# Kernel tuning notes

Hardware: AMD Instinct MI355X
Metric: run time of the kernel (lower is better)

The kernel has to match this reference:

```python
import jax, jax.numpy as jnp
import numpy as np

# Cleaned/faithful JAX port of TATLMPLayer. The original torch code has obvious
# typos (edge_type_feature_embedding used before assignment, self.weight_mlp vs
# self._weight_mlp, missing dim= in concatenate, elementwise mult of (B,E,K) with
# (K,D)); we implement the clearly intended math: two-level masked-softmax
# message passing over an incidence matrix H, gumbel-softmax typed edge
# embeddings, and a 4-head cross-attention to polyline features.

NEG_SLOPE = 0.01  # torch leaky_relu default
TAU = 0.5         # gumbel-softmax temperature 1/2


def _mlp(x, W1, b1, W2, b2):
    return jnp.maximum(x @ W1 + b1, 0.0) @ W2 + b2


def setup_inputs() -> dict:
    B, N, E, P, D, T, K, Hd = 2, 256, 512, 256, 128, 8, 8, 256
    key = jax.random.key(0)
    ks = jax.random.split(key, 40)
    g = lambda i, shape, s=0.05: jax.random.normal(ks[i], shape, dtype=jnp.float32) * s
    return {
        "agent_features": jax.random.normal(ks[0], (B, N, D), dtype=jnp.float32),
        "agent_types": jax.random.uniform(ks[1], (B, N, T), dtype=jnp.float32),
        "polyline_features": jax.random.normal(ks[2], (B, P, D), dtype=jnp.float32),
        "H": (jax.random.uniform(ks[3], (B, E, N)) < 0.1).astype(jnp.float32),
        "type_emb": g(4, (K, D)),
        "w_W1": g(5, (2 * D, Hd)), "w_b1": g(6, (Hd,)), "w_W2": g(7, (Hd, 1)), "w_b2": g(8, (1,)),
        "d_W1": g(9, (D + T, Hd)), "d_b1": g(10, (Hd,)), "d_W2": g(11, (Hd, K)), "d_b2": g(12, (K,)),
        "f_W1": g(13, (D + T, Hd)), "f_b1": g(14, (Hd,)), "f_W2": g(15, (Hd, 1)), "f_b2": g(16, (1,)),
        "o_W1": g(17, (4 * D, Hd)), "o_b1": g(18, (Hd,)), "o_W2": g(19, (Hd, D)), "o_b2": g(20, (D,)),
        "q_W": g(21, (3 * D, D)), "q_b": g(22, (D,)),
        "k_W": g(23, (D, D)), "k_b": g(24, (D,)),
        "v_W": g(25, (D, D)), "v_b": g(26, (D,)),
        "iq_W": g(27, (D, D)), "iq_b": g(28, (D,)),
        "ik_W": g(29, (D, D)), "ik_b": g(30, (D,)),
        "iv_W": g(31, (D, D)), "iv_b": g(32, (D,)),
        "op_W": g(33, (D, D)), "op_b": g(34, (D,)),
    }


def reference(agent_features, agent_types, polyline_features, H, type_emb,
              w_W1, w_b1, w_W2, w_b2, d_W1, d_b1, d_W2, d_b2,
              f_W1, f_b1, f_W2, f_b2, o_W1, o_b1, o_W2, o_b2,
              q_W, q_b, k_W, k_b, v_W, v_b,
              iq_W, iq_b, ik_W, ik_b, iv_W, iv_b, op_W, op_b):
    B, N, D = agent_features.shape
    E = H.shape[1]

    # level 1: incidence-aggregated edge features
    ef_init = jnp.einsum('ben,bnd->bed', H, agent_features)            # (B,E,D)
    pair = jnp.concatenate([
        jnp.broadcast_to(ef_init[:, :, None, :], (B, E, N, D)),
        jnp.broadcast_to(agent_features[:, None, :, :], (B, E, N, D))], axis=-1)
    ew = _mlp(pair, w_W1, w_b1, w_W2, w_b2)[..., 0]                    # (B,E,N)
    Hw = jax.nn.softmax(ew * H, axis=2) * H
    edge_features = jnp.einsum('ben,bnd->bed', Hw, agent_features)     # (B,E,D)

    # typed edge embedding via gumbel-softmax over edge types
    edge_type = jnp.einsum('ben,bnt->bet', H, agent_types)             # (B,E,T)
    et = jnp.concatenate([edge_features, edge_type], axis=-1)          # (B,E,D+T)
    logits = _mlp(et, d_W1, d_b1, d_W2, d_b2)                          # (B,E,K)
    u = jax.random.uniform(jax.random.key(42), logits.shape, minval=1e-6, maxval=1.0 - 1e-6)
    gumbel = -jnp.log(-jnp.log(u))
    distribution = jax.nn.softmax((logits + gumbel) / TAU, axis=-1)
    factor = jax.nn.sigmoid(_mlp(et, f_W1, f_b1, f_W2, f_b2))          # (B,E,1)
    edge_type_embedding = jnp.einsum('bek,kd->bed', factor * distribution, type_emb)

    # level 2: masked edge->agent message passing
    pair2 = jnp.concatenate([
        jnp.broadcast_to(edge_type_embedding[:, :, None, :], (B, E, N, D)),
        jnp.broadcast_to(agent_features[:, None, :, :], (B, E, N, D))], axis=-1)
    pair2 = pair2 * H[..., None]
    hw2 = jnp.where(_mlp(pair2, w_W1, w_b1, w_W2, w_b2)[..., 0] > 0,
                    _mlp(pair2, w_W1, w_b1, w_W2, w_b2)[..., 0], 0.0)
    # leaky relu (single-eval form)
    raw2 = _mlp(pair2, w_W1, w_b1, w_W2, w_b2)[..., 0]
    hw2 = jnp.where(raw2 > 0, raw2, NEG_SLOPE * raw2)                  # (B,E,N)
    Hw2 = jax.nn.softmax(hw2, axis=2) * H
    msg = jnp.einsum('ben,bef->bnf', Hw2,
                     jnp.concatenate([edge_features, edge_type_embedding], axis=-1))
    agent_feat = jnp.concatenate([msg, agent_features], axis=-1)       # (B,N,3D)

    # cross-attention to polylines (4 heads)
    Q = agent_feat @ q_W + q_b
    Kp = polyline_features @ k_W + k_b
    Vp = polyline_features @ v_W + v_b
    q2 = Q @ iq_W + iq_b
    k2 = Kp @ ik_W + ik_b
    v2 = Vp @ iv_W + iv_b
    nh, hd = 4, D // 4
    qh = q2.reshape(B, N, nh, hd)
    kh = k2.reshape(B, -1, nh, hd)
    vh = v2.reshape(B, -1, nh, hd)
    att = jax.nn.softmax(jnp.einsum('bqhd,bkhd->bhqk', qh, kh) / jnp.sqrt(jnp.float32(hd)), axis=-1)
    o = jnp.einsum('bhqk,bkhd->bqhd', att, vh).reshape(B, N, D)
    polyline_new = o @ op_W + op_b                                     # (B,N,D)

    agent_new = _mlp(jnp.concatenate([agent_feat, polyline_new], axis=-1),
                     o_W1, o_b1, o_W2, o_b2)                           # (B,N,D)
    return agent_new, polyline_new
```

## Files before the change

kernel.cpp:

```cpp
#include <hip/hip_runtime.h>
#include <math.h>

#define BB 2
#define NN 256
#define EE 512
#define PP 256
#define DD 128
#define TT 8
#define KK 8
#define HDIM 256

#define WS_G      0
#define WS_C0     8192
#define WS_V      8256
#define WS_U1     139328
#define WS_ETYPE  401472
#define WS_EDGEF  409664
#define WS_ETE    540736
#define WS_HWT    671808
#define WS_K2     933952
#define WS_V2     999488

#define PB_GUM 16
#define PB_INC 272
#define PB_V   528
#define PB_END 784

__device__ inline unsigned rotl32(unsigned x, int d){ return (x<<d)|(x>>(32-d)); }

__device__ inline float bits_to_gumbel(unsigned bits){
  float f = __uint_as_float((bits>>9)|0x3f800000u) - 1.0f;
  const float minv = 1e-6f;
  const float maxv = 1.0f - 1e-6f;
  float u = f*(maxv-minv) + minv;
  u = fmaxf(minv, u);
  return -logf(-logf(u));
}

__device__ __forceinline__ void f4fma(float4& a, float x, const float4& w){
  a.x += x*w.x; a.y += x*w.y; a.z += x*w.z; a.w += x*w.w;
}

__device__ __forceinline__ void block_reduce2_sum(float v[2], float* wred){
  int lane = threadIdx.x & 63, wid = threadIdx.x >> 6;
  #pragma unroll
  for (int s=32;s>0;s>>=1){
    #pragma unroll
    for (int r=0;r<2;r++){ v[r] += __shfl_xor(v[r], s, 64); }
  }
  if (lane==0){
    #pragma unroll
    for (int r=0;r<2;r++) wred[wid*2+r]=v[r];
  }
  __syncthreads();
  #pragma unroll
  for (int r=0;r<2;r++)
    v[r] = (wred[0*2+r]+wred[1*2+r]) + (wred[2*2+r]+wred[3*2+r]);
  __syncthreads();
}

__device__ __forceinline__ void mlp128_lds2(const float (*in)[DD], const float* W, const float* bias,
                                            float (*outl)[DD], float* part, int t){
  int c=(t&31)*4, ks=t>>5;
  float4 a[2];
  #pragma unroll
  for (int r=0;r<2;r++) a[r]=make_float4(0.f,0.f,0.f,0.f);
  #pragma unroll 4
  for (int i=ks*16;i<ks*16+16;i++){
    float4 w = *(const float4*)&W[(size_t)i*DD+c];
    #pragma unroll
    for (int r=0;r<2;r++) f4fma(a[r], in[r][i], w);
  }
  #pragma unroll
  for (int r=0;r<2;r++) *(float4*)&part[(ks*2+r)*DD+c]=a[r];
  __syncthreads();
  int cc=t&127, r=t>>7;
  {
    float s=0.f;
    #pragma unroll
    for (int k2=0;k2<8;k2++) s+=part[(k2*2+r)*DD+cc];
    outl[r][cc]=s+bias[cc];
  }
  __syncthreads();
}

__device__ __forceinline__ void mlp128_glob2(const float (*in)[DD], const float* W, const float* bias,
                                             float* dst, int r0, float* part, int t){
  int c=(t&31)*4, ks=t>>5;
  float4 a[2];
  #pragma unroll
  for (int r=0;r<2;r++) a[r]=make_float4(0.f,0.f,0.f,0.f);
  #pragma unroll 4
  for (int i=ks*16;i<ks*16+16;i++){
    float4 w = *(const float4*)&W[(size_t)i*DD+c];
    #pragma unroll
    for (int r=0;r<2;r++) f4fma(a[r], in[r][i], w);
  }
  #pragma unroll
  for (int r=0;r<2;r++) *(float4*)&part[(ks*2+r)*DD+c]=a[r];
  __syncthreads();
  int cc=t&127, r=t>>7;
  {
    float s=0.f;
    #pragma unroll
    for (int k2=0;k2<8;k2++) s+=part[(k2*2+r)*DD+cc];
    dst[(size_t)(r0+r)*DD+cc]=s+bias[cc];
  }
  __syncthreads();
}

__global__ void prep_kernel(float* g, float* c0, const float* w_b1,
                            const float* w_W2, const float* w_b2,
                            const float* Hm, const float* af, const float* at,
                            const float* wW1, const float* wb1,
                            float* U1g, float* etype_g, float* Vout,
                            const float* pf,
                            const float* kW, const float* kb, const float* ikW, const float* ikb,
                            const float* vW, const float* vb, const float* ivW, const float* ivb,
                            float* k2, float* v2){
  __shared__ float part[4096];
  __shared__ float wred[16];
  __shared__ int   hcomp[4*256];
  __shared__ int   hcnt[4];
  __shared__ float ef[4][DD];
  __shared__ float xs[2][DD];
  __shared__ float bufB[2][DD];
  int blk = blockIdx.x;
  int t = threadIdx.x;
  int lane = t & 63, wid = t >> 6;

  if (blk < PB_GUM){
    int j = blk*256 + t;
    {
      const unsigned k0=0u, k1=42u;
      const unsigned ks2 = k0^k1^0x1BD11BDAu;
      unsigned x0 = (unsigned)j, x1 = (unsigned)j + 4096u;
      const int r0_[4]={13,15,26,6}, r1_[4]={17,29,16,24};
      x0 += k0; x1 += k1;
      #pragma unroll
      for(int i=0;i<4;i++){ x0+=x1; x1=rotl32(x1,r0_[i]); x1^=x0; }
      x0+=k1; x1+=ks2+1u;
      #pragma unroll
      for(int i=0;i<4;i++){ x0+=x1; x1=rotl32(x1,r1_[i]); x1^=x0; }
      x0+=ks2; x1+=k0+2u;
      #pragma unroll
      for(int i=0;i<4;i++){ x0+=x1; x1=rotl32(x1,r0_[i]); x1^=x0; }
      x0+=k0; x1+=k1+3u;
      #pragma unroll
      for(int i=0;i<4;i++){ x0+=x1; x1=rotl32(x1,r1_[i]); x1^=x0; }
      x0+=k1; x1+=ks2+4u;
      #pragma unroll
      for(int i=0;i<4;i++){ x0+=x1; x1=rotl32(x1,r0_[i]); x1^=x0; }
      x0+=ks2; x1+=k0+5u;
      g[j]      = bits_to_gumbel(x0);
      g[j+4096] = bits_to_gumbel(x1);
    }
    if (blk == 0){
      float v4[2];
      v4[0] = fmaxf(w_b1[t],0.f)*w_W2[t]; v4[1]=0.f;
      block_reduce2_sum(v4, wred);
      if (t==0) c0[0] = v4[0] + w_b2[0];
    }
  } else if (blk < PB_INC){
    int e0 = (blk - PB_GUM)*4;
    int b = e0 >> 9;
    {
      int r = wid;
      const float* Hrow = Hm + (size_t)(e0+r)*NN;
      int base = 0;
      #pragma unroll
      for (int c4=0;c4<4;c4++){
        int n2 = c4*64 + lane;
        bool pred = (Hrow[n2] != 0.f);
        unsigned long long mask = __ballot(pred);
        int off = __popcll(mask & ((1ull<<lane)-1ull));
        if (pred) hcomp[r*256+base+off] = n2;
        base += __popcll(mask);
      }
      if (lane==0) hcnt[r] = base;
    }
    __syncthreads();
    {
      int d = t & 127, eh = t >> 7;
      #pragma unroll
      for (int rr=0;rr<2;rr++){
        int r = eh*2 + rr;
        int tot = hcnt[r];
        float a = 0.f, a2 = 0.f;
        for (int i=0;i<tot;i++){
          int n2 = hcomp[r*256+i];
          a += af[((size_t)b*NN+n2)*DD + d];
          if (d < TT) a2 += at[((size_t)b*NN+n2)*TT + d];
        }
        ef[r][d] = a;
        if (d < TT) etype_g[(size_t)(e0+r)*TT + d] = a2;
      }
    }
    __syncthreads();
    {
      int c = (t&63)*4, ks = t>>6;
      float4 acc[4];
      #pragma unroll
      for (int r=0;r<4;r++) acc[r]=make_float4(0.f,0.f,0.f,0.f);
      #pragma unroll 8
      for (int i=ks*32; i<ks*32+32; i++){
        float4 w = *(const float4*)&wW1[(size_t)i*HDIM + c];
        #pragma unroll
        for (int r=0;r<4;r++) f4fma(acc[r], ef[r][i], w);
      }
      #pragma unroll
      for (int r=0;r<4;r++) *(float4*)&part[(ks*4+r)*HDIM + c] = acc[r];
    }
    __syncthreads();
    {
      float bv = wb1[t];
      #pragma unroll
      for (int r=0;r<4;r++){
        float s = (part[(0*4+r)*HDIM+t] + part[(1*4+r)*HDIM+t])
                + (part[(2*4+r)*HDIM+t] + part[(3*4+r)*HDIM+t]);
        U1g[(size_t)(e0+r)*HDIM + t] = s + bv;
      }
    }
  } else if (blk < PB_V){
    int r0 = (blk - PB_INC)*2;
    const float* W = wW1 + (size_t)DD*HDIM;
    for (int i=t;i<2*DD;i+=256) xs[i>>7][i&127] = af[(size_t)(r0+(i>>7))*DD + (i&127)];
    __syncthreads();
    int c = (t&63)*4, ks = t>>6;
    float4 acc[2];
    #pragma unroll
    for (int r=0;r<2;r++) acc[r]=make_float4(0.f,0.f,0.f,0.f);
    #pragma unroll 8
    for (int i=ks*32; i<ks*32+32; i++){
      float4 w = *(const float4*)&W[(size_t)i*HDIM + c];
      #pragma unroll
      for (int r=0;r<2;r++) f4fma(acc[r], xs[r][i], w);
    }
    #pragma unroll
    for (int r=0;r<2;r++) *(float4*)&part[(ks*2+r)*HDIM + c] = acc[r];
    __syncthreads();
    #pragma unroll
    for (int r=0;r<2;r++){
      float s = (part[(0*2+r)*HDIM+t] + part[(1*2+r)*HDIM+t])
              + (part[(2*2+r)*HDIM+t] + part[(3*2+r)*HDIM+t]);
      Vout[(size_t)(r0+r)*HDIM + t] = s;
    }
  } else {
    int r0 = (blk - PB_V)*2;
    for (int i=t;i<2*DD;i+=256) xs[i>>7][i&127] = pf[(size_t)(r0+(i>>7))*DD + (i&127)];
    __syncthreads();
    mlp128_lds2 (xs, kW, kb, bufB, part, t);
    mlp128_glob2(bufB, ikW, ikb, k2, r0, part, t);
    mlp128_lds2 (xs, vW, vb, bufB, part, t);
    mlp128_glob2(bufB, ivW, ivb, v2, r0, part, t);
  }
}

__global__ __launch_bounds__(512) void edge_kernel(
                            const float* Hm, const float* af,
                            const float* Vm, const float* U1g, const float* etype_g,
                            const float* wW1, const float* wb1, const float* wW2, const float* wb2,
                            const float* dW1, const float* db1, const float* dW2, const float* db2,
                            const float* fW1, const float* fb1, const float* fW2, const float* fb2,
                            const float* type_emb, const float* g, const float* c0p,
                            float* edgef_g, float* ete_g, float* HwT){
  __shared__ float bufA[8192];
  __shared__ float w2s[HDIM*KK];
  __shared__ float w2l[HDIM];
  __shared__ float et4[4][144];
  __shared__ float hd4[4][HDIM];
  __shared__ float redsm[512];
  __shared__ float wred[16];
  __shared__ float fdv[4][KK];
  __shared__ int   hcnt[4];
  __shared__ int   hcomp[4*256];

  int e0 = blockIdx.x*4;
  int b  = e0 >> 9;
  int t  = threadIdx.x;
  int lane = t & 63, wid = t >> 6;

  int cW=(t&63)*4, ksW=t>>6;
  float4 wreg[16];
  #pragma unroll
  for (int i=0;i<16;i++)
    wreg[i] = *(const float4*)&wW1[(size_t)(ksW*16+i)*HDIM + cW];

  if (t < HDIM) w2l[t] = wW2[t];
  for (int i=t;i<HDIM*KK;i+=512) w2s[i] = dW2[i];
  {
    int h=t&255, rh=t>>8;
    #pragma unroll
    for (int rr=0;rr<2;rr++){
      int r = 2*rh+rr;
      hd4[r][h] = U1g[(size_t)(e0+r)*HDIM + h];
    }
  }
  if (t < 32){ int r=t>>3, j=t&7; et4[r][DD+j] = etype_g[(size_t)(e0+r)*TT + j]; }
  if (wid < 4){
    int r = wid;
    const float* Hrow = Hm + (size_t)(e0+r)*NN;
    int base = 0;
    #pragma unroll
    for (int c4=0;c4<4;c4++){
      int n2 = c4*64 + lane;
      bool pred = (Hrow[n2] != 0.f);
      unsigned long long mask = __ballot(pred);
      int off = __popcll(mask & ((1ull<<lane)-1ull));
      if (pred) hcomp[r*256+base+off] = n2;
      base += __popcll(mask);
    }
    if (lane==0) hcnt[r] = base;
  }
  __syncthreads();
  {
    int n = t&255, hh = t>>8;
    const float4* Vrow = (const float4*)(Vm + ((size_t)(b*NN)+n)*HDIM);
    float acc[4]={0.f,0.f,0.f,0.f};
    #pragma unroll 4
    for (int ii=hh*32; ii<hh*32+32; ii++){
      float4 v = Vrow[ii];
      float w0=w2l[4*ii+0], w1=w2l[4*ii+1], wc=w2l[4*ii+2], w3=w2l[4*ii+3];
      #pragma unroll
      for (int r=0;r<4;r++){
        acc[r] += fmaxf(hd4[r][4*ii+0]+v.x,0.f)*w0
                + fmaxf(hd4[r][4*ii+1]+v.y,0.f)*w1
                + fmaxf(hd4[r][4*ii+2]+v.z,0.f)*wc
                + fmaxf(hd4[r][4*ii+3]+v.w,0.f)*w3;
      }
    }
    #pragma unroll
    for (int r=0;r<4;r++) bufA[(hh*4+r)*256 + n] = acc[r];
  }
  __syncthreads();
  if (wid < 4){
    int r = wid;
    float b2v = wb2[0];
    float x[4]; bool msk[4];
    #pragma unroll
    for (int q=0;q<4;q++){
      int n = lane + 64*q;
      msk[q] = (Hm[(size_t)(e0+r)*NN + n] != 0.f);
      x[q] = msk[q] ? (bufA[(0*4+r)*256+n] + bufA[(1*4+r)*256+n] + b2v) : 0.f;
    }
    float m = fmaxf(fmaxf(x[0],x[1]), fmaxf(x[2],x[3]));
    #pragma unroll
    for (int s2=32;s2>0;s2>>=1) m = fmaxf(m, __shfl_xor(m, s2, 64));
    float p[4]; float ss=0.f;
    #pragma unroll
    for (int q=0;q<4;q++){ p[q]=expf(x[q]-m); ss+=p[q]; }
    #pragma unroll
    for (int s2=32;s2>0;s2>>=1) ss += __shfl_xor(ss, s2, 64);
    float inv = 1.f/ss;
    #pragma unroll
    for (int q=0;q<4;q++){
      int n = lane + 64*q;
      bufA[3072 + r*256 + n] = msk[q] ? p[q]*inv : 0.f;
    }
  }
  __syncthreads();
  {
    int d = t & 127, r = t >> 7;
    int tot = hcnt[r];
    float a = 0.f;
    for (int i=0;i<tot;i++){
      int n2 = hcomp[r*256+i];
      a += bufA[3072 + r*256 + n2] * af[((size_t)b*NN+n2)*DD + d];
    }
    et4[r][d] = a;
    edgef_g[(size_t)(e0+r)*DD + d] = a;
  }
  __syncthreads();
  {
    int half = t>>8, tt = t&255;
    int c=(tt&63)*4, ks=tt>>6;
    const float* W = half ? fW1 : dW1;
    float4 acc[4];
    #pragma unroll
    for (int r=0;r<4;r++) acc[r]=make_float4(0.f,0.f,0.f,0.f);
    #pragma unroll 4
    for (int i=ks*34;i<ks*34+34;i++){
      float4 w = *(const float4*)&W[(size_t)i*HDIM+c];
      #pragma unroll
      for (int r=0;r<4;r++) f4fma(acc[r], et4[r][i], w);
    }
    #pragma unroll
    for (int r=0;r<4;r++) *(float4*)&bufA[half*4096 + (ks*4+r)*HDIM + c] = acc[r];
  }
  __syncthreads();
  {
    int h=t&255, rh=t>>8;
    float bd = db1[h], bf = fb1[h], fw = fW2[h];
    float val[2];
    #pragma unroll
    for (int rr=0;rr<2;rr++){
      int r = 2*rh+rr;
      float sd=0.f, sf=0.f;
      #pragma unroll
      for (int k=0;k<4;k++){ sd += bufA[(k*4+r)*HDIM+h]; sf += bufA[4096+(k*4+r)*HDIM+h]; }
      hd4[r][h] = fmaxf(sd+bd, 0.f);
      val[rr] = fmaxf(sf+bf, 0.f)*fw;
    }
    #pragma unroll
    for (int s2=32;s2>0;s2>>=1){
      val[0] += __shfl_xor(val[0], s2, 64);
      val[1] += __shfl_xor(val[1], s2, 64);
    }
    if (lane==0){ wred[wid*2]=val[0]; wred[wid*2+1]=val[1]; }
  }
  __syncthreads();
  {
    int r_ = t>>7, rem = t&127, k_ = rem&7, j_ = rem>>3;
    float lp = 0.f;
    #pragma unroll 4
    for (int i=0;i<16;i++){
      int h = j_ + 16*i;
      lp += hd4[r_][h]*w2s[h*KK + k_];
    }
    redsm[t] = lp;
  }
  __syncthreads();
  if (wid == 0 && lane < 32){
    int r = lane>>3, k = lane&7;
    int base = (r>=2)?4:0, off = r&1;
    float fs = 0.f;
    #pragma unroll
    for (int w=0;w<4;w++) fs += wred[(base+w)*2 + off];
    float fac = 1.f/(1.f+expf(-(fs+fb2[0])));
    float s = db2[k] + g[(size_t)(e0+r)*KK + k];
    #pragma unroll
    for (int j=0;j<16;j++) s += redsm[r*128 + j*8 + k];
    float z = s*2.0f;
    float m = z;
    m = fmaxf(m, __shfl_xor(m, 1, 64));
    m = fmaxf(m, __shfl_xor(m, 2, 64));
    m = fmaxf(m, __shfl_xor(m, 4, 64));
    float pz = expf(z - m);
    float sum = pz;
    sum += __shfl_xor(sum, 1, 64);
    sum += __shfl_xor(sum, 2, 64);
    sum += __shfl_xor(sum, 4, 64);
    fdv[r][k] = fac * pz / sum;
  }
  __syncthreads();
  {
    int d = t&127, r = t>>7;
    float a = 0.f;
    #pragma unroll
    for (int k=0;k<KK;k++) a += fdv[r][k]*type_emb[(size_t)k*DD + d];
    et4[r][d] = a;
    ete_g[(size_t)(e0+r)*DD + d] = a;
  }
  __syncthreads();
  {
    float4 acc[4];
    #pragma unroll
    for (int r=0;r<4;r++) acc[r]=make_float4(0.f,0.f,0.f,0.f);
    #pragma unroll
    for (int i=0;i<16;i++){
      int idx = ksW*16 + i;
      #pragma unroll
      for (int r=0;r<4;r++) f4fma(acc[r], et4[r][idx], wreg[i]);
    }
    #pragma unroll
    for (int r=0;r<4;r++) *(float4*)&bufA[(ksW*4+r)*HDIM + cW] = acc[r];
  }
  __syncthreads();
  {
    int h=t&255, rh=t>>8;
    float bv = wb1[h];
    #pragma unroll
    for (int rr=0;rr<2;rr++){
      int r = 2*rh+rr;
      float s=0.f;
      #pragma unroll
      for (int k=0;k<8;k++) s += bufA[(k*4+r)*HDIM + h];
      hd4[r][h] = s + bv;
    }
  }
  __syncthreads();
  {
    int n = t&255, hh = t>>8;
    const float4* Vrow = (const float4*)(Vm + ((size_t)(b*NN)+n)*HDIM);
    float acc[4]={0.f,0.f,0.f,0.f};
    #pragma unroll 4
    for (int ii=hh*32; ii<hh*32+32; ii++){
      float4 v = Vrow[ii];
      float w0=w2l[4*ii+0], w1=w2l[4*ii+1], wc=w2l[4*ii+2], w3=w2l[4*ii+3];
      #pragma unroll
      for (int r=0;r<4;r++){
        acc[r] += fmaxf(hd4[r][4*ii+0]+v.x,0.f)*w0
                + fmaxf(hd4[r][4*ii+1]+v.y,0.f)*w1
                + fmaxf(hd4[r][4*ii+2]+v.z,0.f)*wc
                + fmaxf(hd4[r][4*ii+3]+v.w,0.f)*w3;
      }
    }
    #pragma unroll
    for (int r=0;r<4;r++) bufA[(hh*4+r)*256 + n] = acc[r];
  }
  __syncthreads();
  if (wid < 4){
    int r = wid;
    float b2v = wb2[0];
    float c0 = c0p[0];
    float x[4]; bool msk[4];
    #pragma unroll
    for (int q=0;q<4;q++){
      int n = lane + 64*q;
      msk[q] = (Hm[(size_t)(e0+r)*NN + n] != 0.f);
      float raw = msk[q] ? (bufA[(0*4+r)*256+n] + bufA[(1*4+r)*256+n] + b2v) : c0;
      x[q] = raw>0.f ? raw : 0.01f*raw;
    }
    float m = fmaxf(fmaxf(x[0],x[1]), fmaxf(x[2],x[3]));
    #pragma unroll
    for (int s2=32;s2>0;s2>>=1) m = fmaxf(m, __shfl_xor(m, s2, 64));
    float p[4]; float ss=0.f;
    #pragma unroll
    for (int q=0;q<4;q++){ p[q]=expf(x[q]-m); ss+=p[q]; }
    #pragma unroll
    for (int s2=32;s2>0;s2>>=1) ss += __shfl_xor(ss, s2, 64);
    float inv = 1.f/ss;
    #pragma unroll
    for (int q=0;q<4;q++){
      int n = lane + 64*q;
      bufA[2048 + r*256 + n] = msk[q] ? p[q]*inv : 0.f;
    }
  }
  __syncthreads();
  if (t < 256){
    int n = t;
    float4 o4;
    o4.x = bufA[2048 + 0*256 + n];
    o4.y = bufA[2048 + 1*256 + n];
    o4.z = bufA[2048 + 2*256 + n];
    o4.w = bufA[2048 + 3*256 + n];
    int eb = e0 & 511;
    *(float4*)(HwT + ((size_t)(b*NN)+n)*EE + eb) = o4;
  }
}

__global__ __launch_bounds__(512) void agent_kernel(
                             const float* HwT, const float* edgef, const float* ete,
                             const float* af,
                             const float* qW, const float* qb, const float* iqW, const float* iqb,
                             const float* k2, const float* v2,
                             const float* op_W, const float* op_b,
                             const float* oW1, const float* ob1,
                             const float* oW2, const float* ob2,
                             float* pnew, float* anew){
  __shared__ int   ecomp[2][EE];
  __shared__ float wcomp[2][EE];
  __shared__ int   wcnt[2][4];
  __shared__ float agfl[2][512];
  __shared__ float part[4096];
  __shared__ float Qs[2][DD];
  __shared__ float qr[2][DD];
  __shared__ float att[2][4][PP+1];
  __shared__ float o_l[2][DD];
  __shared__ float hid[2][HDIM];
  int n0 = blockIdx.x*2; int b = n0 >> 8; int t = threadIdx.x;
  int tt = t & 255, rr = t >> 8;
  int lane = t & 63, wid = t >> 6;
  int lw = tt >> 6;

  {
    int bn = n0 + rr;
    const float* wrow = HwT + (size_t)bn*EE;
    int total = 0;
    #pragma unroll
    for (int p=0;p<2;p++){
      int e = p*256 + tt;
      float w = wrow[e];
      bool pred = (w != 0.f);
      unsigned long long mask = __ballot(pred);
      if (lane==0) wcnt[rr][lw] = __popcll(mask);
      int off = __popcll(mask & ((1ull<<lane)-1ull));
      __syncthreads();
      int wb = total;
      for (int ww=0; ww<lw; ww++) wb += wcnt[rr][ww];
      if (pred){ ecomp[rr][wb+off] = e; wcomp[rr][wb+off] = w; }
      total += wcnt[rr][0]+wcnt[rr][1]+wcnt[rr][2]+wcnt[rr][3];
      __syncthreads();
    }
    float acc = 0.f;
    const float* srcbase = (tt < DD) ? (edgef + (size_t)b*EE*DD + tt)
                                     : (ete   + (size_t)b*EE*DD + (tt-DD));
    for (int i=0;i<total;i++){
      acc += wcomp[rr][i] * srcbase[(size_t)ecomp[rr][i]*DD];
    }
    agfl[rr][tt] = acc;
    if (tt < DD) agfl[rr][2*DD+tt] = af[(size_t)bn*DD + tt];
  }
  __syncthreads();
  int c=(tt&31)*4, ps=tt>>5;
  {
    float4 a = make_float4(0.f,0.f,0.f,0.f);
    #pragma unroll 4
    for (int i=ps*48;i<ps*48+48;i++){
      float4 w = *(const float4*)&qW[(size_t)i*DD+c];
      f4fma(a, agfl[rr][i], w);
    }
    *(float4*)&part[(rr*8+ps)*DD+c]=a;
  }
  __syncthreads();
  if (t<256){
    int cc=t&127, r=t>>7;
    float s=0.f;
    #pragma unroll
    for (int k=0;k<8;k++) s+=part[(r*8+k)*DD+cc];
    Qs[r][cc]=s+qb[cc];
  }
  __syncthreads();
  {
    float4 a = make_float4(0.f,0.f,0.f,0.f);
    #pragma unroll 4
    for (int i=ps*16;i<ps*16+16;i++){
      float4 w = *(const float4*)&iqW[(size_t)i*DD+c];
      f4fma(a, Qs[rr][i], w);
    }
    *(float4*)&part[(rr*8+ps)*DD+c]=a;
  }
  __syncthreads();
  if (t<256){
    int cc=t&127, r=t>>7;
    float s=0.f;
    #pragma unroll
    for (int k=0;k<8;k++) s+=part[(r*8+k)*DD+cc];
    qr[r][cc]=s+iqb[cc];
  }
  __syncthreads();
  const float scale = 0.17677669529663687f;
  {
    const float* krow = k2 + ((size_t)(b*PP) + tt)*DD;
    #pragma unroll
    for (int hh=0;hh<2;hh++){
      int h = rr*2+hh;
      const float4* k4 = (const float4*)(krow + h*32);
      float s0=0.f, s1=0.f;
      #pragma unroll
      for (int jj=0;jj<8;jj++){
        float4 kk = k4[jj];
        s0 += qr[0][h*32+jj*4+0]*kk.x + qr[0][h*32+jj*4+1]*kk.y
            + qr[0][h*32+jj*4+2]*kk.z + qr[0][h*32+jj*4+3]*kk.w;
        s1 += qr[1][h*32+jj*4+0]*kk.x + qr[1][h*32+jj*4+1]*kk.y
            + qr[1][h*32+jj*4+2]*kk.z + qr[1][h*32+jj*4+3]*kk.w;
      }
      att[0][h][tt] = s0*scale;
      att[1][h][tt] = s1*scale;
    }
  }
  __syncthreads();
  {
    int r = wid>>2, h = wid&3;
    float v0 = att[r][h][lane],     v1 = att[r][h][lane+64],
          ve = att[r][h][lane+128], v3 = att[r][h][lane+192];
    float m = fmaxf(fmaxf(v0,v1), fmaxf(ve,v3));
    #pragma unroll
    for (int s2=32;s2>0;s2>>=1) m = fmaxf(m, __shfl_xor(m, s2, 64));
    float e0 = expf(v0-m), e1 = expf(v1-m), e2 = expf(ve-m), e3 = expf(v3-m);
    float ss = (e0+e1)+(e2+e3);
    #pragma unroll
    for (int s2=32;s2>0;s2>>=1) ss += __shfl_xor(ss, s2, 64);
    float inv = 1.f/ss;
    att[r][h][lane] = e0*inv; att[r][h][lane+64] = e1*inv;
    att[r][h][lane+128] = e2*inv; att[r][h][lane+192] = e3*inv;
  }
  __syncthreads();
  int h2 = c >> 5;
  {
    float4 acc = make_float4(0.f,0.f,0.f,0.f);
    #pragma unroll 4
    for (int i=0;i<32;i++){
      int p = ps*32+i;
      float4 v = *(const float4*)&v2[((size_t)(b*PP)+p)*DD + c];
      f4fma(acc, att[rr][h2][p], v);
    }
    *(float4*)&part[(rr*8+ps)*DD+c]=acc;
  }
  __syncthreads();
  if (t<256){
    int cc=t&127, r=t>>7;
    float s=0.f;
    #pragma unroll
    for (int k=0;k<8;k++) s+=part[(r*8+k)*DD+cc];
    o_l[r][cc]=s;
  }
  __syncthreads();
  {
    float4 a2 = make_float4(0.f,0.f,0.f,0.f);
    #pragma unroll 4
    for (int i=ps*16;i<ps*16+16;i++){
      float4 w = *(const float4*)&op_W[(size_t)i*DD + c];
      f4fma(a2, o_l[rr][i], w);
    }
    *(float4*)&part[(rr*8+ps)*DD+c]=a2;
  }
  __syncthreads();
  if (t<256){
    int cc=t&127, r=t>>7;
    float s=0.f;
    #pragma unroll
    for (int k=0;k<8;k++) s+=part[(r*8+k)*DD+cc];
    float pv = s+op_b[cc];
    agfl[r][3*DD+cc] = pv;
    pnew[(size_t)(n0+r)*DD+cc] = pv;
  }
  __syncthreads();
  {
    int c1=(t&63)*4, ks1=t>>6;
    float4 acc[2];
    #pragma unroll
    for (int r=0;r<2;r++) acc[r]=make_float4(0.f,0.f,0.f,0.f);
    #pragma unroll 8
    for (int i=ks1*64;i<ks1*64+64;i++){
      float4 w = *(const float4*)&oW1[(size_t)i*HDIM+c1];
      f4fma(acc[0], agfl[0][i], w);
      f4fma(acc[1], agfl[1][i], w);
    }
    #pragma unroll
    for (int r=0;r<2;r++) *(float4*)&part[(ks1*2+r)*HDIM+c1]=acc[r];
  }
  __syncthreads();
  {
    int h=t&255, r=t>>8;
    float s=0.f;
    #pragma unroll
    for (int k=0;k<8;k++) s+=part[(k*2+r)*HDIM+h];
    hid[r][h] = fmaxf(s+ob1[h], 0.f);
  }
  __syncthreads();
  {
    float4 a2 = make_float4(0.f,0.f,0.f,0.f);
    #pragma unroll 8
    for (int h=ps*32;h<ps*32+32;h++){
      float4 w = *(const float4*)&oW2[(size_t)h*DD+c];
      f4fma(a2, hid[rr][h], w);
    }
    *(float4*)&part[(rr*8+ps)*DD+c]=a2;
  }
  __syncthreads();
  if (t<256){
    int cc=t&127, r=t>>7;
    float s=0.f;
    #pragma unroll
    for (int k=0;k<8;k++) s+=part[(r*8+k)*DD+cc];
    anew[(size_t)(n0+r)*DD+cc]=s+ob2[cc];
  }
}

extern "C" void kernel_launch(void* const* d_in, const int* in_sizes, int n_in,
                              void* d_out, int out_size, void* d_ws, size_t ws_size,
                              hipStream_t stream) {
  const float* af       = (const float*)d_in[0];
  const float* at       = (const float*)d_in[1];
  const float* pf       = (const float*)d_in[2];
  const float* Hm       = (const float*)d_in[3];
  const float* type_emb = (const float*)d_in[4];
  const float* w_W1 = (const float*)d_in[5];
  const float* w_b1 = (const float*)d_in[6];
  const float* w_W2 = (const float*)d_in[7];
  const float* w_b2 = (const float*)d_in[8];
  const float* d_W1 = (const float*)d_in[9];
  const float* d_b1 = (const float*)d_in[10];
  const float* d_W2 = (const float*)d_in[11];
  const float* d_b2 = (const float*)d_in[12];
  const float* f_W1 = (const float*)d_in[13];
  const float* f_b1 = (const float*)d_in[14];
  const float* f_W2 = (const float*)d_in[15];
  const float* f_b2 = (const float*)d_in[16];
  const float* o_W1 = (const float*)d_in[17];
  const float* o_b1 = (const float*)d_in[18];
  const float* o_W2 = (const float*)d_in[19];
  const float* o_b2 = (const float*)d_in[20];
  const float* q_W  = (const float*)d_in[21];
  const float* q_b  = (const float*)d_in[22];
  const float* k_W  = (const float*)d_in[23];
  const float* k_b  = (const float*)d_in[24];
  const float* v_W  = (const float*)d_in[25];
  const float* v_b  = (const float*)d_in[26];
  const float* iq_W = (const float*)d_in[27];
  const float* iq_b = (const float*)d_in[28];
  const float* ik_W = (const float*)d_in[29];
  const float* ik_b = (const float*)d_in[30];
  const float* iv_W = (const float*)d_in[31];
  const float* iv_b = (const float*)d_in[32];
  const float* op_W = (const float*)d_in[33];
  const float* op_b = (const float*)d_in[34];

  float* ws   = (float*)d_ws;
  float* out  = (float*)d_out;
  float* anew = out;
  float* pnew = out + BB*NN*DD;

  prep_kernel<<<PB_END, 256, 0, stream>>>(
      ws+WS_G, ws+WS_C0, w_b1, w_W2, w_b2,
      Hm, af, at, w_W1, w_b1,
      ws+WS_U1, ws+WS_ETYPE, ws+WS_V,
      pf, k_W,k_b,ik_W,ik_b, v_W,v_b,iv_W,iv_b,
      ws+WS_K2, ws+WS_V2);
  edge_kernel<<<256,512,0,stream>>>(
      Hm, af, ws+WS_V, ws+WS_U1, ws+WS_ETYPE,
      w_W1, w_b1, w_W2, w_b2,
      d_W1,d_b1,d_W2,d_b2, f_W1,f_b1,f_W2,f_b2,
      type_emb, ws+WS_G, ws+WS_C0,
      ws+WS_EDGEF, ws+WS_ETE, ws+WS_HWT);
  agent_kernel<<<256,512,0,stream>>>(
      ws+WS_HWT, ws+WS_EDGEF, ws+WS_ETE, af,
      q_W, q_b, iq_W, iq_b,
      ws+WS_K2, ws+WS_V2, op_W, op_b,
      o_W1,o_b1,o_W2,o_b2, pnew, anew);
}
```

Measured before the change: 89.08 us.

## Fuse three kernels into one persistent kernel with atomic grid barriers

```diff
diff --git a/kernel.cpp b/kernel.cpp
--- a/kernel.cpp
+++ b/kernel.cpp
@@ -10,21 +10,13 @@
 #define KK 8
 #define HDIM 256
 
-#define WS_G      0
-#define WS_C0     8192
-#define WS_V      8256
-#define WS_U1     139328
-#define WS_ETYPE  401472
-#define WS_EDGEF  409664
-#define WS_ETE    540736
-#define WS_HWT    671808
-#define WS_K2     933952
-#define WS_V2     999488
-
-#define PB_GUM 16
-#define PB_INC 272
-#define PB_V   528
-#define PB_END 784
+#define WS_V      0
+#define WS_EDGEF  131072
+#define WS_ETE    262144
+#define WS_HWT    393216
+#define WS_K2     655360
+#define WS_V2     720896
+#define WS_CNT    786432
 
 __device__ inline unsigned rotl32(unsigned x, int d){ return (x<<d)|(x>>(32-d)); }
 
@@ -41,97 +33,80 @@
   a.x += x*w.x; a.y += x*w.y; a.z += x*w.z; a.w += x*w.w;
 }
 
-__device__ __forceinline__ void block_reduce2_sum(float v[2], float* wred){
-  int lane = threadIdx.x & 63, wid = threadIdx.x >> 6;
-  #pragma unroll
-  for (int s=32;s>0;s>>=1){
-    #pragma unroll
-    for (int r=0;r<2;r++){ v[r] += __shfl_xor(v[r], s, 64); }
-  }
-  if (lane==0){
-    #pragma unroll
-    for (int r=0;r<2;r++) wred[wid*2+r]=v[r];
+__device__ __forceinline__ void grid_sync(int* cnt, int target){
+  __syncthreads();
+  if (threadIdx.x == 0){
+    __threadfence();
+    atomicAdd(cnt, 1);
+    while (__hip_atomic_load(cnt, __ATOMIC_ACQUIRE, __HIP_MEMORY_SCOPE_AGENT) < target){
+      __builtin_amdgcn_s_sleep(8);
+    }
   }
   __syncthreads();
-  #pragma unroll
-  for (int r=0;r<2;r++)
-    v[r] = (wred[0*2+r]+wred[1*2+r]) + (wred[2*2+r]+wred[3*2+r]);
+  __threadfence();
+}
+
+__device__ __forceinline__ void mlp128x2_512(const float* inA, const float* inB,
+      const float* W, const float* bias, float* outA, float* outB, float* part, int t){
+  int c=(t&31)*4, ks=t>>5;
+  float4 a0=make_float4(0.f,0.f,0.f,0.f), a1=a0;
+  #pragma unroll 4
+  for (int i=ks*8;i<ks*8+8;i++){
+    float4 w = *(const float4*)&W[(size_t)i*DD+c];
+    f4fma(a0, inA[i], w); f4fma(a1, inB[i], w);
+  }
+  *(float4*)&part[(ks*2+0)*DD+c]=a0;
+  *(float4*)&part[(ks*2+1)*DD+c]=a1;
   __syncthreads();
-}
-
-__device__ __forceinline__ void mlp128_lds2(const float (*in)[DD], const float* W, const float* bias,
-                                            float (*outl)[DD], float* part, int t){
-  int c=(t&31)*4, ks=t>>5;
-  float4 a[2];
-  #pragma unroll
-  for (int r=0;r<2;r++) a[r]=make_float4(0.f,0.f,0.f,0.f);
-  #pragma unroll 4
-  for (int i=ks*16;i<ks*16+16;i++){
-    float4 w = *(const float4*)&W[(size_t)i*DD+c];
-    #pragma unroll
-    for (int r=0;r<2;r++) f4fma(a[r], in[r][i], w);
-  }
-  #pragma unroll
-  for (int r=0;r<2;r++) *(float4*)&part[(ks*2+r)*DD+c]=a[r];
-  __syncthreads();
-  int cc=t&127, r=t>>7;
-  {
+  if (t < 256){
+    int cc=t&127, r=t>>7;
     float s=0.f;
     #pragma unroll
-    for (int k2=0;k2<8;k2++) s+=part[(k2*2+r)*DD+cc];
-    outl[r][cc]=s+bias[cc];
+    for (int k=0;k<16;k++) s+=part[(k*2+r)*DD+cc];
+    float val = s + bias[cc];
+    if (r==0) outA[cc]=val; else outB[cc]=val;
   }
   __syncthreads();
 }
 
-__device__ __forceinline__ void mlp128_glob2(const float (*in)[DD], const float* W, const float* bias,
-                                             float* dst, int r0, float* part, int t){
-  int c=(t&31)*4, ks=t>>5;
-  float4 a[2];
-  #pragma unroll
-  for (int r=0;r<2;r++) a[r]=make_float4(0.f,0.f,0.f,0.f);
-  #pragma unroll 4
-  for (int i=ks*16;i<ks*16+16;i++){
-    float4 w = *(const float4*)&W[(size_t)i*DD+c];
-    #pragma unroll
-    for (int r=0;r<2;r++) f4fma(a[r], in[r][i], w);
-  }
-  #pragma unroll
-  for (int r=0;r<2;r++) *(float4*)&part[(ks*2+r)*DD+c]=a[r];
-  __syncthreads();
-  int cc=t&127, r=t>>7;
-  {
-    float s=0.f;
-    #pragma unroll
-    for (int k2=0;k2<8;k2++) s+=part[(k2*2+r)*DD+cc];
-    dst[(size_t)(r0+r)*DD+cc]=s+bias[cc];
-  }
-  __syncthreads();
-}
-
-__global__ void prep_kernel(float* g, float* c0, const float* w_b1,
-                            const float* w_W2, const float* w_b2,
-                            const float* Hm, const float* af, const float* at,
-                            const float* wW1, const float* wb1,
-                            float* U1g, float* etype_g, float* Vout,
-                            const float* pf,
-                            const float* kW, const float* kb, const float* ikW, const float* ikb,
-                            const float* vW, const float* vb, const float* ivW, const float* ivb,
-                            float* k2, float* v2){
-  __shared__ float part[4096];
-  __shared__ float wred[16];
-  __shared__ int   hcomp[4*256];
-  __shared__ int   hcnt[4];
-  __shared__ float ef[4][DD];
-  __shared__ float xs[2][DD];
-  __shared__ float bufB[2][DD];
+__global__ __launch_bounds__(512) void fused_kernel(
+    const float* af, const float* at, const float* pf, const float* Hm,
+    const float* type_emb,
+    const float* wW1, const float* wb1, const float* wW2, const float* wb2,
+    const float* dW1, const float* db1, const float* dW2, const float* db2,
+    const float* fW1, const float* fb1, const float* fW2, const float* fb2,
+    const float* oW1, const float* ob1, const float* oW2, const float* ob2,
+    const float* qW,  const float* qb,  const float* kW,  const float* kb,
+    const float* vW,  const float* vb,  const float* iqW, const float* iqb,
+    const float* ikW, const float* ikb, const float* ivW, const float* ivb,
+    const float* opW, const float* opb,
+    float* Vg, float* edgef_g, float* ete_g, float* HwT,
+    float* k2g, float* v2g, int* cnt,
+    float* pnew, float* anew){
+
+  __shared__ float pool[11712];
+  __shared__ float hd4s[4*HDIM];
+  __shared__ int   hcompS[4*256];
+  __shared__ int   hcntS[4];
+  __shared__ float etloc[4*TT];
+  __shared__ float gloc[32];
+  __shared__ float wredS[16];
+  __shared__ float mredS[4], sinvS[4];
+  __shared__ float c0s;
+  __shared__ float fdvS[4*KK];
+
   int blk = blockIdx.x;
   int t = threadIdx.x;
   int lane = t & 63, wid = t >> 6;
 
-  if (blk < PB_GUM){
-    int j = blk*256 + t;
-    {
+  {
+    float* partA = pool;
+    float* ef    = pool + 8192;
+    float* xsA   = pool + 8704;
+    float* bufB  = pool + 8960;
+
+    if (t < 32){
+      int j = (blk < 128) ? (blk*32 + t) : ((blk-128)*32 + t);
       const unsigned k0=0u, k1=42u;
       const unsigned ks2 = k0^k1^0x1BD11BDAu;
       unsigned x0 = (unsigned)j, x1 = (unsigned)j + 4096u;
@@ -152,19 +127,20 @@
       #pragma unroll
       for(int i=0;i<4;i++){ x0+=x1; x1=rotl32(x1,r0_[i]); x1^=x0; }
       x0+=ks2; x1+=k0+5u;
-      g[j]      = bits_to_gumbel(x0);
-      g[j+4096] = bits_to_gumbel(x1);
-    }
-    if (blk == 0){
-      float v4[2];
-      v4[0] = fmaxf(w_b1[t],0.f)*w_W2[t]; v4[1]=0.f;
-      block_reduce2_sum(v4, wred);
-      if (t==0) c0[0] = v4[0] + w_b2[0];
-    }
-  } else if (blk < PB_INC){
-    int e0 = (blk - PB_GUM)*4;
-    int b = e0 >> 9;
-    {
+      gloc[t] = bits_to_gumbel((blk<128)? x0 : x1);
+    }
+    if (t < 256){
+      float v = fmaxf(wb1 ? 0.f : 0.f, 0.f);
+    }
+    if (t < 256){
+      float v = fmaxf(wb1[t],0.f)*wW2[t];
+      #pragma unroll
+      for (int s=32;s>0;s>>=1) v += __shfl_xor(v, s, 64);
+      if (lane==0) wredS[wid] = v;
+    }
+    int e0 = blk*4;
+    int b  = e0 >> 9;
+    if (wid < 4){
       int r = wid;
       const float* Hrow = Hm + (size_t)(e0+r)*NN;
       int base = 0;
@@ -174,577 +150,538 @@
         bool pred = (Hrow[n2] != 0.f);
         unsigned long long mask = __ballot(pred);
         int off = __popcll(mask & ((1ull<<lane)-1ull));
-        if (pred) hcomp[r*256+base+off] = n2;
+        if (pred) hcompS[r*256+base+off] = n2;
         base += __popcll(mask);
       }
-      if (lane==0) hcnt[r] = base;
-    }
-    __syncthreads();
-    {
-      int d = t & 127, eh = t >> 7;
+      if (lane==0) hcntS[r] = base;
+    }
+    __syncthreads();
+    if (t==0) c0s = wredS[0]+wredS[1]+wredS[2]+wredS[3] + wb2[0];
+    {
+      int d = t & 127, r = t >> 7;
+      int tot = hcntS[r];
+      float a = 0.f, a2 = 0.f;
+      for (int i=0;i<tot;i++){
+        int n2 = hcompS[r*256+i];
+        a += af[((size_t)b*NN+n2)*DD + d];
+        if (d < TT) a2 += at[((size_t)b*NN+n2)*TT + d];
+      }
+      ef[r*DD+d] = a;
+      if (d < TT) etloc[r*TT+d] = a2;
+    }
+    __syncthreads();
+    {
+      int c=(t&63)*4, ks=t>>6;
+      float4 acc[4];
+      #pragma unroll
+      for (int r=0;r<4;r++) acc[r]=make_float4(0.f,0.f,0.f,0.f);
+      #pragma unroll 4
+      for (int i=ks*16; i<ks*16+16; i++){
+        float4 w = *(const float4*)&wW1[(size_t)i*HDIM + c];
+        #pragma unroll
+        for (int r=0;r<4;r++) f4fma(acc[r], ef[r*DD+i], w);
+      }
+      #pragma unroll
+      for (int r=0;r<4;r++) *(float4*)&partA[(ks*4+r)*HDIM + c] = acc[r];
+    }
+    __syncthreads();
+    {
+      int h=t&255, rh=t>>8;
+      float bv = wb1[h];
       #pragma unroll
       for (int rr=0;rr<2;rr++){
-        int r = eh*2 + rr;
-        int tot = hcnt[r];
-        float a = 0.f, a2 = 0.f;
-        for (int i=0;i<tot;i++){
-          int n2 = hcomp[r*256+i];
-          a += af[((size_t)b*NN+n2)*DD + d];
-          if (d < TT) a2 += at[((size_t)b*NN+n2)*TT + d];
+        int r = 2*rh+rr;
+        float s=0.f;
+        #pragma unroll
+        for (int k=0;k<8;k++) s += partA[(k*4+r)*HDIM + h];
+        hd4s[r*HDIM+h] = s + bv;
+      }
+    }
+    __syncthreads();
+    {
+      int r0v = blk*2;
+      const float* W = wW1 + (size_t)DD*HDIM;
+      for (int i=t;i<2*DD;i+=512) xsA[i] = af[(size_t)(r0v+(i>>7))*DD + (i&127)];
+      __syncthreads();
+      int c=(t&63)*4, ks=t>>6;
+      float4 a0=make_float4(0.f,0.f,0.f,0.f), a1=a0;
+      #pragma unroll 4
+      for (int i=ks*16; i<ks*16+16; i++){
+        float4 w = *(const float4*)&W[(size_t)i*HDIM + c];
+        f4fma(a0, xsA[i], w); f4fma(a1, xsA[DD+i], w);
+      }
+      *(float4*)&partA[(ks*2+0)*HDIM + c] = a0;
+      *(float4*)&partA[(ks*2+1)*HDIM + c] = a1;
+      __syncthreads();
+      {
+        int h=t&255, r=t>>8;
+        float s=0.f;
+        #pragma unroll
+        for (int k=0;k<8;k++) s += partA[(k*2+r)*HDIM + h];
+        Vg[(size_t)(r0v+r)*HDIM + h] = s;
+      }
+      __syncthreads();
+    }
+    {
+      int r0p = blk*2;
+      for (int i=t;i<2*DD;i+=512) xsA[i] = pf[(size_t)(r0p+(i>>7))*DD + (i&127)];
+      __syncthreads();
+      mlp128x2_512(xsA, xsA+DD, kW, kb, bufB, bufB+DD, partA, t);
+      mlp128x2_512(bufB, bufB+DD, ikW, ikb,
+                   k2g + (size_t)r0p*DD, k2g + (size_t)(r0p+1)*DD, partA, t);
+      mlp128x2_512(xsA, xsA+DD, vW, vb, bufB, bufB+DD, partA, t);
+      mlp128x2_512(bufB, bufB+DD, ivW, ivb,
+                   v2g + (size_t)r0p*DD, v2g + (size_t)(r0p+1)*DD, partA, t);
+    }
+  }
+  grid_sync(cnt + 0, 256);
+
+  {
+    float* bufA = pool;
+    float* w2s  = pool + 8192;
+    float* w2l  = pool + 10240;
+    float* et4  = pool + 10496;
+    float* redsm= pool + 11072;
+
+    int e0 = blk*4;
+    int b  = e0 >> 9;
+
+    int cW=(t&63)*4, ksW=t>>6;
+    float4 wreg[16];
+    #pragma unroll
+    for (int i=0;i<16;i++)
+      wreg[i] = *(const float4*)&wW1[(size_t)(ksW*16+i)*HDIM + cW];
+
+    if (t < HDIM) w2l[t] = wW2[t];
+    for (int i=t;i<HDIM*KK;i+=512) w2s[i] = dW2[i];
+    if (t < 32){ int r=t>>3, j=t&7; et4[r*144+DD+j] = etloc[r*TT+j]; }
+    __syncthreads();
+    {
+      int n = t&255, hh = t>>8;
+      const float4* Vrow = (const float4*)(Vg + ((size_t)(b*NN)+n)*HDIM);
+      float acc[4]={0.f,0.f,0.f,0.f};
+      #pragma unroll 4
+      for (int ii=hh*32; ii<hh*32+32; ii++){
+        float4 v = Vrow[ii];
+        float w0=w2l[4*ii+0], w1=w2l[4*ii+1], wc=w2l[4*ii+2], w3=w2l[4*ii+3];
+        #pragma unroll
+        for (int r=0;r<4;r++){
+          acc[r] += fmaxf(hd4s[r*HDIM+4*ii+0]+v.x,0.f)*w0
+                  + fmaxf(hd4s[r*HDIM+4*ii+1]+v.y,0.f)*w1
+                  + fmaxf(hd4s[r*HDIM+4*ii+2]+v.z,0.f)*wc
+                  + fmaxf(hd4s[r*HDIM+4*ii+3]+v.w,0.f)*w3;
         }
-        ef[r][d] = a;
-        if (d < TT) etype_g[(size_t)(e0+r)*TT + d] = a2;
-      }
-    }
-    __syncthreads();
-    {
-      int c = (t&63)*4, ks = t>>6;
+      }
+      #pragma unroll
+      for (int r=0;r<4;r++) bufA[(hh*4+r)*256 + n] = acc[r];
+    }
+    __syncthreads();
+    if (wid < 4){
+      int r = wid;
+      float b2v = wb2[0];
+      float x[4]; bool msk[4];
+      #pragma unroll
+      for (int q=0;q<4;q++){
+        int n = lane + 64*q;
+        msk[q] = (Hm[(size_t)(e0+r)*NN + n] != 0.f);
+        x[q] = msk[q] ? (bufA[(0*4+r)*256+n] + bufA[(1*4+r)*256+n] + b2v) : 0.f;
+      }
+      float m = fmaxf(fmaxf(x[0],x[1]), fmaxf(x[2],x[3]));
+      #pragma unroll
+      for (int s2=32;s2>0;s2>>=1) m = fmaxf(m, __shfl_xor(m, s2, 64));
+      float p[4]; float ss=0.f;
+      #pragma unroll
+      for (int q=0;q<4;q++){ p[q]=expf(x[q]-m); ss+=p[q]; }
+      #pragma unroll
+      for (int s2=32;s2>0;s2>>=1) ss += __shfl_xor(ss, s2, 64);
+      float inv = 1.f/ss;
+      #pragma unroll
+      for (int q=0;q<4;q++){
+        int n = lane + 64*q;
+        bufA[3072 + r*256 + n] = msk[q] ? p[q]*inv : 0.f;
+      }
+    }
+    __syncthreads();
+    {
+      int d = t & 127, r = t >> 7;
+      int tot = hcntS[r];
+      float a = 0.f;
+      for (int i=0;i<tot;i++){
+        int n2 = hcompS[r*256+i];
+        a += bufA[3072 + r*256 + n2] * af[((size_t)b*NN+n2)*DD + d];
+      }
+      et4[r*144+d] = a;
+      edgef_g[(size_t)(e0+r)*DD + d] = a;
+    }
+    __syncthreads();
+    {
+      int half = t>>8, tt2 = t&255;
+      int c=(tt2&63)*4, ks=tt2>>6;
+      const float* W = half ? fW1 : dW1;
       float4 acc[4];
       #pragma unroll
       for (int r=0;r<4;r++) acc[r]=make_float4(0.f,0.f,0.f,0.f);
+      #pragma unroll 4
+      for (int i=ks*34;i<ks*34+34;i++){
+        float4 w = *(const float4*)&W[(size_t)i*HDIM+c];
+        #pragma unroll
+        for (int r=0;r<4;r++) f4fma(acc[r], et4[r*144+i], w);
+      }
+      #pragma unroll
+      for (int r=0;r<4;r++) *(float4*)&bufA[half*4096 + (ks*4+r)*HDIM + c] = acc[r];
+    }
+    __syncthreads();
+    {
+      int h=t&255, rh=t>>8;
+      float bd = db1[h], bf = fb1[h], fw = fW2[h];
+      float val[2];
+      #pragma unroll
+      for (int rr=0;rr<2;rr++){
+        int r = 2*rh+rr;
+        float sd=0.f, sf=0.f;
+        #pragma unroll
+        for (int k=0;k<4;k++){ sd += bufA[(k*4+r)*HDIM+h]; sf += bufA[4096+(k*4+r)*HDIM+h]; }
+        hd4s[r*HDIM+h] = fmaxf(sd+bd, 0.f);
+        val[rr] = fmaxf(sf+bf, 0.f)*fw;
+      }
+      #pragma unroll
+      for (int s2=32;s2>0;s2>>=1){
+        val[0] += __shfl_xor(val[0], s2, 64);
+        val[1] += __shfl_xor(val[1], s2, 64);
+      }
+      if (lane==0){ wredS[wid*2]=val[0]; wredS[wid*2+1]=val[1]; }
+    }
+    __syncthreads();
+    {
+      int r_ = t>>7, rem = t&127, k_ = rem&7, j_ = rem>>3;
+      float lp = 0.f;
+      #pragma unroll 4
+      for (int i=0;i<16;i++){
+        int h = j_ + 16*i;
+        lp += hd4s[r_*HDIM+h]*w2s[h*KK + k_];
+      }
+      redsm[t] = lp;
+    }
+    __syncthreads();
+    if (wid == 0 && lane < 32){
+      int r = lane>>3, k = lane&7;
+      int base = (r>=2)?4:0, off = r&1;
+      float fs = 0.f;
+      #pragma unroll
+      for (int w=0;w<4;w++) fs += wredS[(base+w)*2 + off];
+      float fac = 1.f/(1.f+expf(-(fs+fb2[0])));
+      float s = db2[k] + gloc[r*8+k];
+      #pragma unroll
+      for (int j=0;j<16;j++) s += redsm[r*128 + j*8 + k];
+      float z = s*2.0f;
+      float m = z;
+      m = fmaxf(m, __shfl_xor(m, 1, 64));
+      m = fmaxf(m, __shfl_xor(m, 2, 64));
+      m = fmaxf(m, __shfl_xor(m, 4, 64));
+      float pz = expf(z - m);
+      float sum = pz;
+      sum += __shfl_xor(sum, 1, 64);
+      sum += __shfl_xor(sum, 2, 64);
+      sum += __shfl_xor(sum, 4, 64);
+      fdvS[r*KK+k] = fac * pz / sum;
+    }
+    __syncthreads();
+    {
+      int d = t&127, r = t>>7;
+      float a = 0.f;
+      #pragma unroll
+      for (int k=0;k<KK;k++) a += fdvS[r*KK+k]*type_emb[(size_t)k*DD + d];
+      et4[r*144+d] = a;
+      ete_g[(size_t)(e0+r)*DD + d] = a;
+    }
+    __syncthreads();
+    {
+      float4 acc[4];
+      #pragma unroll
+      for (int r=0;r<4;r++) acc[r]=make_float4(0.f,0.f,0.f,0.f);
+      #pragma unroll
+      for (int i=0;i<16;i++){
+        int idx = ksW*16 + i;
+        #pragma unroll
+        for (int r=0;r<4;r++) f4fma(acc[r], et4[r*144+idx], wreg[i]);
+      }
+      #pragma unroll
+      for (int r=0;r<4;r++) *(float4*)&bufA[(ksW*4+r)*HDIM + cW] = acc[r];
+    }
+    __syncthreads();
+    {
+      int h=t&255, rh=t>>8;
+      float bv = wb1[h];
+      #pragma unroll
+      for (int rr=0;rr<2;rr++){
+        int r = 2*rh+rr;
+        float s=0.f;
+        #pragma unroll
+        for (int k=0;k<8;k++) s += bufA[(k*4+r)*HDIM + h];
+        hd4s[r*HDIM+h] = s + bv;
+      }
+    }
+    __syncthreads();
+    {
+      int n = t&255, hh = t>>8;
+      const float4* Vrow = (const float4*)(Vg + ((size_t)(b*NN)+n)*HDIM);
+      float acc[4]={0.f,0.f,0.f,0.f};
+      #pragma unroll 4
+      for (int ii=hh*32; ii<hh*32+32; ii++){
+        float4 v = Vrow[ii];
+        float w0=w2l[4*ii+0], w1=w2l[4*ii+1], wc=w2l[4*ii+2], w3=w2l[4*ii+3];
+        #pragma unroll
+        for (int r=0;r<4;r++){
+          acc[r] += fmaxf(hd4s[r*HDIM+4*ii+0]+v.x,0.f)*w0
+                  + fmaxf(hd4s[r*HDIM+4*ii+1]+v.y,0.f)*w1
+                  + fmaxf(hd4s[r*HDIM+4*ii+2]+v.z,0.f)*wc
+                  + fmaxf(hd4s[r*HDIM+4*ii+3]+v.w,0.f)*w3;
+        }
+      }
+      #pragma unroll
+      for (int r=0;r<4;r++) bufA[(hh*4+r)*256 + n] = acc[r];
+    }
+    __syncthreads();
+    if (wid < 4){
+      int r = wid;
+      float b2v = wb2[0];
+      float c0 = c0s;
+      float x[4]; bool msk[4];
+      #pragma unroll
+      for (int q=0;q<4;q++){
+        int n = lane + 64*q;
+        msk[q] = (Hm[(size_t)(e0+r)*NN + n] != 0.f);
+        float raw = msk[q] ? (bufA[(0*4+r)*256+n] + bufA[(1*4+r)*256+n] + b2v) : c0;
+        x[q] = raw>0.f ? raw : 0.01f*raw;
+      }
+      float m = fmaxf(fmaxf(x[0],x[1]), fmaxf(x[2],x[3]));
+      #pragma unroll
+      for (int s2=32;s2>0;s2>>=1) m = fmaxf(m, __shfl_xor(m, s2, 64));
+      float p[4]; float ss=0.f;
+      #pragma unroll
+      for (int q=0;q<4;q++){ p[q]=expf(x[q]-m); ss+=p[q]; }
+      #pragma unroll
+      for (int s2=32;s2>0;s2>>=1) ss += __shfl_xor(ss, s2, 64);
+      float inv = 1.f/ss;
+      #pragma unroll
+      for (int q=0;q<4;q++){
+        int n = lane + 64*q;
+        bufA[2048 + r*256 + n] = msk[q] ? p[q]*inv : 0.f;
+      }
+    }
+    __syncthreads();
+    if (t < 256){
+      int n = t;
+      float4 o4;
+      o4.x = bufA[2048 + 0*256 + n];
+      o4.y = bufA[2048 + 1*256 + n];
+      o4.z = bufA[2048 + 2*256 + n];
+      o4.w = bufA[2048 + 3*256 + n];
+      int eb = e0 & 511;
+      *(float4*)(HwT + ((size_t)(b*NN)+n)*EE + eb) = o4;
+    }
+  }
+  grid_sync(cnt + 1, 256);
+
+  {
+    int*   ecompC = (int*)pool;
+    float* wcompC = pool + 1024;
+    int*   wcntC  = (int*)(pool + 2048);
+    float* agflC  = pool + 2064;
+    float* partC  = pool + 3088;
+    float* QsC    = pool + 7184;
+    float* qrC    = pool + 7440;
+    float* attC   = pool + 7696;
+    float* olC    = pool + 9752;
+    float* hidC   = pool + 10008;
+
+    int n0 = blk*2; int b = n0 >> 8;
+    int tt = t & 255, rr = t >> 8;
+    int lw = tt >> 6;
+
+    {
+      int bn = n0 + rr;
+      const float* wrow = HwT + (size_t)bn*EE;
+      int total = 0;
+      #pragma unroll
+      for (int p=0;p<2;p++){
+        int e = p*256 + tt;
+        float w = wrow[e];
+        bool pred = (w != 0.f);
+        unsigned long long mask = __ballot(pred);
+        if (lane==0) wcntC[rr*4+lw] = __popcll(mask);
+        int off = __popcll(mask & ((1ull<<lane)-1ull));
+        __syncthreads();
+        int wb = total;
+        for (int ww=0; ww<lw; ww++) wb += wcntC[rr*4+ww];
+        if (pred){ ecompC[rr*512+wb+off] = e; wcompC[rr*512+wb+off] = w; }
+        total += wcntC[rr*4+0]+wcntC[rr*4+1]+wcntC[rr*4+2]+wcntC[rr*4+3];
+        __syncthreads();
+      }
+      float acc = 0.f;
+      const float* srcbase = (tt < DD) ? (edgef_g + (size_t)b*EE*DD + tt)
+                                       : (ete_g   + (size_t)b*EE*DD + (tt-DD));
+      for (int i=0;i<total;i++){
+        acc += wcompC[rr*512+i] * srcbase[(size_t)ecompC[rr*512+i]*DD];
+      }
+      agflC[rr*512+tt] = acc;
+      if (tt < DD) agflC[rr*512+2*DD+tt] = af[(size_t)bn*DD + tt];
+    }
+    __syncthreads();
+    int c=(tt&31)*4, ps=tt>>5;
+    {
+      float4 a = make_float4(0.f,0.f,0.f,0.f);
+      #pragma unroll 4
+      for (int i=ps*48;i<ps*48+48;i++){
+        float4 w = *(const float4*)&qW[(size_t)i*DD+c];
+        f4fma(a, agflC[rr*512+i], w);
+      }
+      *(float4*)&partC[(rr*8+ps)*DD+c]=a;
+    }
+    __syncthreads();
+    if (t<256){
+      int cc=t&127, r=t>>7;
+      float s=0.f;
+      #pragma unroll
+      for (int k=0;k<8;k++) s+=partC[(r*8+k)*DD+cc];
+      QsC[r*DD+cc]=s+qb[cc];
+    }
+    __syncthreads();
+    {
+      float4 a = make_float4(0.f,0.f,0.f,0.f);
+      #pragma unroll 4
+      for (int i=ps*16;i<ps*16+16;i++){
+        float4 w = *(const float4*)&iqW[(size_t)i*DD+c];
+        f4fma(a, QsC[rr*DD+i], w);
+      }
+      *(float4*)&partC[(rr*8+ps)*DD+c]=a;
+    }
+    __syncthreads();
+    if (t<256){
+      int cc=t&127, r=t>>7;
+      float s=0.f;
+      #pragma unroll
+      for (int k=0;k<8;k++) s+=partC[(r*8+k)*DD+cc];
+      qrC[r*DD+cc]=s+iqb[cc];
+    }
+    __syncthreads();
+    const float scale = 0.17677669529663687f;
+    {
+      const float* krow = k2g + ((size_t)(b*PP) + tt)*DD;
+      #pragma unroll
+      for (int hh=0;hh<2;hh++){
+        int h = rr*2+hh;
+        const float4* k4 = (const float4*)(krow + h*32);
+        float s0=0.f, s1=0.f;
+        #pragma unroll
+        for (int jj=0;jj<8;jj++){
+          float4 kk = k4[jj];
+          s0 += qrC[0*DD+h*32+jj*4+0]*kk.x + qrC[0*DD+h*32+jj*4+1]*kk.y
+              + qrC[0*DD+h*32+jj*4+2]*kk.z + qrC[0*DD+h*32+jj*4+3]*kk.w;
+          s1 += qrC[1*DD+h*32+jj*4+0]*kk.x + qrC[1*DD+h*32+jj*4+1]*kk.y
+              + qrC[1*DD+h*32+jj*4+2]*kk.z + qrC[1*DD+h*32+jj*4+3]*kk.w;
+        }
+        attC[(0*4+h)*257+tt] = s0*scale;
+        attC[(1*4+h)*257+tt] = s1*scale;
+      }
+    }
+    __syncthreads();
+    {
+      int r = wid>>2, h = wid&3;
+      float* a = attC + (r*4+h)*257;
+      float v0 = a[lane], v1 = a[lane+64], ve = a[lane+128], v3 = a[lane+192];
+      float m = fmaxf(fmaxf(v0,v1), fmaxf(ve,v3));
+      #pragma unroll
+      for (int s2=32;s2>0;s2>>=1) m = fmaxf(m, __shfl_xor(m, s2, 64));
+      float e0_ = expf(v0-m), e1 = expf(v1-m), e2 = expf(ve-m), e3 = expf(v3-m);
+      float ss = (e0_+e1)+(e2+e3);
+      #pragma unroll
+      for (int s2=32;s2>0;s2>>=1) ss += __shfl_xor(ss, s2, 64);
+      float inv = 1.f/ss;
+      a[lane] = e0_*inv; a[lane+64] = e1*inv;
+      a[lane+128] = e2*inv; a[lane+192] = e3*inv;
+    }
+    __syncthreads();
+    int h2 = c >> 5;
+    {
+      float4 acc = make_float4(0.f,0.f,0.f,0.f);
+      #pragma unroll 4
+      for (int i=0;i<32;i++){
+        int p = ps*32+i;
+        float4 v = *(const float4*)&v2g[((size_t)(b*PP)+p)*DD + c];
+        f4fma(acc, attC[(rr*4+h2)*257+p], v);
+      }
+      *(float4*)&partC[(rr*8+ps)*DD+c]=acc;
+    }
+    __syncthreads();
+    if (t<256){
+      int cc=t&127, r=t>>7;
+      float s=0.f;
+      #pragma unroll
+      for (int k=0;k<8;k++) s+=partC[(r*8+k)*DD+cc];
+      olC[r*DD+cc]=s;
+    }
+    __syncthreads();
+    {
+      float4 a2 = make_float4(0.f,0.f,0.f,0.f);
+      #pragma unroll 4
+      for (int i=ps*16;i<ps*16+16;i++){
+        float4 w = *(const float4*)&opW[(size_t)i*DD + c];
+        f4fma(a2, olC[rr*DD+i], w);
+      }
+      *(float4*)&partC[(rr*8+ps)*DD+c]=a2;
+    }
+    __syncthreads();
+    if (t<256){
+      int cc=t&127, r=t>>7;
+      float s=0.f;
+      #pragma unroll
+      for (int k=0;k<8;k++) s+=partC[(r*8+k)*DD+cc];
+      float pv = s+opb[cc];
+      agflC[r*512+3*DD+cc] = pv;
+      pnew[(size_t)(n0+r)*DD+cc] = pv;
+    }
+    __syncthreads();
+    {
+      int c1=(t&63)*4, ks1=t>>6;
+      float4 acc[2];
+      #pragma unroll
+      for (int r=0;r<2;r++) acc[r]=make_float4(0.f,0.f,0.f,0.f);
       #pragma unroll 8
-      for (int i=ks*32; i<ks*32+32; i++){
-        float4 w = *(const float4*)&wW1[(size_t)i*HDIM + c];
-        #pragma unroll
-        for (int r=0;r<4;r++) f4fma(acc[r], ef[r][i], w);
-      }
-      #pragma unroll
-      for (int r=0;r<4;r++) *(float4*)&part[(ks*4+r)*HDIM + c] = acc[r];
-    }
-    __syncthreads();
-    {
-      float bv = wb1[t];
-      #pragma unroll
-      for (int r=0;r<4;r++){
-        float s = (part[(0*4+r)*HDIM+t] + part[(1*4+r)*HDIM+t])
-                + (part[(2*4+r)*HDIM+t] + part[(3*4+r)*HDIM+t]);
-        U1g[(size_t)(e0+r)*HDIM + t] = s + bv;
-      }
-    }
-  } else if (blk < PB_V){
-    int r0 = (blk - PB_INC)*2;
-    const float* W = wW1 + (size_t)DD*HDIM;
-    for (int i=t;i<2*DD;i+=256) xs[i>>7][i&127] = af[(size_t)(r0+(i>>7))*DD + (i&127)];
-    __syncthreads();
-    int c = (t&63)*4, ks = t>>6;
-    float4 acc[2];
-    #pragma unroll
-    for (int r=0;r<2;r++) acc[r]=make_float4(0.f,0.f,0.f,0.f);
-    #pragma unroll 8
-    for (int i=ks*32; i<ks*32+32; i++){
-      float4 w = *(const float4*)&W[(size_t)i*HDIM + c];
-      #pragma unroll
-      for (int r=0;r<2;r++) f4fma(acc[r], xs[r][i], w);
-    }
-    #pragma unroll
-    for (int r=0;r<2;r++) *(float4*)&part[(ks*2+r)*HDIM + c] = acc[r];
-    __syncthreads();
-    #pragma unroll
-    for (int r=0;r<2;r++){
-      float s = (part[(0*2+r)*HDIM+t] + part[(1*2+r)*HDIM+t])
-              + (part[(2*2+r)*HDIM+t] + part[(3*2+r)*HDIM+t]);
-      Vout[(size_t)(r0+r)*HDIM + t] = s;
-    }
-  } else {
-    int r0 = (blk - PB_V)*2;
-    for (int i=t;i<2*DD;i+=256) xs[i>>7][i&127] = pf[(size_t)(r0+(i>>7))*DD + (i&127)];
-    __syncthreads();
-    mlp128_lds2 (xs, kW, kb, bufB, part, t);
-    mlp128_glob2(bufB, ikW, ikb, k2, r0, part, t);
-    mlp128_lds2 (xs, vW, vb, bufB, part, t);
-    mlp128_glob2(bufB, ivW, ivb, v2, r0, part, t);
-  }
-}
-
-__global__ __launch_bounds__(512) void edge_kernel(
-                            const float* Hm, const float* af,
-                            const float* Vm, const float* U1g, const float* etype_g,
-                            const float* wW1, const float* wb1, const float* wW2, const float* wb2,
-                            const float* dW1, const float* db1, const float* dW2, const float* db2,
-                            const float* fW1, const float* fb1, const float* fW2, const float* fb2,
-                            const float* type_emb, const float* g, const float* c0p,
-                            float* edgef_g, float* ete_g, float* HwT){
-  __shared__ float bufA[8192];
-  __shared__ float w2s[HDIM*KK];
-  __shared__ float w2l[HDIM];
-  __shared__ float et4[4][144];
-  __shared__ float hd4[4][HDIM];
-  __shared__ float redsm[512];
-  __shared__ float wred[16];
-  __shared__ float fdv[4][KK];
-  __shared__ int   hcnt[4];
-  __shared__ int   hcomp[4*256];
-
-  int e0 = blockIdx.x*4;
-  int b  = e0 >> 9;
-  int t  = threadIdx.x;
-  int lane = t & 63, wid = t >> 6;
-
-  int cW=(t&63)*4, ksW=t>>6;
-  float4 wreg[16];
-  #pragma unroll
-  for (int i=0;i<16;i++)
-    wreg[i] = *(const float4*)&wW1[(size_t)(ksW*16+i)*HDIM + cW];
-
-  if (t < HDIM) w2l[t] = wW2[t];
-  for (int i=t;i<HDIM*KK;i+=512) w2s[i] = dW2[i];
-  {
-    int h=t&255, rh=t>>8;
-    #pragma unroll
-    for (int rr=0;rr<2;rr++){
-      int r = 2*rh+rr;
-      hd4[r][h] = U1g[(size_t)(e0+r)*HDIM + h];
-    }
-  }
-  if (t < 32){ int r=t>>3, j=t&7; et4[r][DD+j] = etype_g[(size_t)(e0+r)*TT + j]; }
-  if (wid < 4){
-    int r = wid;
-    const float* Hrow = Hm + (size_t)(e0+r)*NN;
-    int base = 0;
-    #pragma unroll
-    for (int c4=0;c4<4;c4++){
-      int n2 = c4*64 + lane;
-      bool pred = (Hrow[n2] != 0.f);
-      unsigned long long mask = __ballot(pred);
-      int off = __popcll(mask & ((1ull<<lane)-1ull));
-      if (pred) hcomp[r*256+base+off] = n2;
-      base += __popcll(mask);
-    }
-    if (lane==0) hcnt[r] = base;
-  }
-  __syncthreads();
-  {
-    int n = t&255, hh = t>>8;
-    const float4* Vrow = (const float4*)(Vm + ((size_t)(b*NN)+n)*HDIM);
-    float acc[4]={0.f,0.f,0.f,0.f};
-    #pragma unroll 4
-    for (int ii=hh*32; ii<hh*32+32; ii++){
-      float4 v = Vrow[ii];
-      float w0=w2l[4*ii+0], w1=w2l[4*ii+1], wc=w2l[4*ii+2], w3=w2l[4*ii+3];
-      #pragma unroll
-      for (int r=0;r<4;r++){
-        acc[r] += fmaxf(hd4[r][4*ii+0]+v.x,0.f)*w0
-                + fmaxf(hd4[r][4*ii+1]+v.y,0.f)*w1
-                + fmaxf(hd4[r][4*ii+2]+v.z,0.f)*wc
-                + fmaxf(hd4[r][4*ii+3]+v.w,0.f)*w3;
-      }
-    }
-    #pragma unroll
-    for (int r=0;r<4;r++) bufA[(hh*4+r)*256 + n] = acc[r];
-  }
-  __syncthreads();
-  if (wid < 4){
-    int r = wid;
-    float b2v = wb2[0];
-    float x[4]; bool msk[4];
-    #pragma unroll
-    for (int q=0;q<4;q++){
-      int n = lane + 64*q;
-      msk[q] = (Hm[(size_t)(e0+r)*NN + n] != 0.f);
-      x[q] = msk[q] ? (bufA[(0*4+r)*256+n] + bufA[(1*4+r)*256+n] + b2v) : 0.f;
-    }
-    float m = fmaxf(fmaxf(x[0],x[1]), fmaxf(x[2],x[3]));
-    #pragma unroll
-    for (int s2=32;s2>0;s2>>=1) m = fmaxf(m, __shfl_xor(m, s2, 64));
-    float p[4]; float ss=0.f;
-    #pragma unroll
-    for (int q=0;q<4;q++){ p[q]=expf(x[q]-m); ss+=p[q]; }
-    #pragma unroll
-    for (int s2=32;s2>0;s2>>=1) ss += __shfl_xor(ss, s2, 64);
-    float inv = 1.f/ss;
-    #pragma unroll
-    for (int q=0;q<4;q++){
-      int n = lane + 64*q;
-      bufA[3072 + r*256 + n] = msk[q] ? p[q]*inv : 0.f;
-    }
-  }
-  __syncthreads();
-  {
-    int d = t & 127, r = t >> 7;
-    int tot = hcnt[r];
-    float a = 0.f;
-    for (int i=0;i<tot;i++){
-      int n2 = hcomp[r*256+i];
-      a += bufA[3072 + r*256 + n2] * af[((size_t)b*NN+n2)*DD + d];
-    }
-    et4[r][d] = a;
-    edgef_g[(size_t)(e0+r)*DD + d] = a;
-  }
-  __syncthreads();
-  {
-    int half = t>>8, tt = t&255;
-    int c=(tt&63)*4, ks=tt>>6;
-    const float* W = half ? fW1 : dW1;
-    float4 acc[4];
-    #pragma unroll
-    for (int r=0;r<4;r++) acc[r]=make_float4(0.f,0.f,0.f,0.f);
-    #pragma unroll 4
-    for (int i=ks*34;i<ks*34+34;i++){
-      float4 w = *(const float4*)&W[(size_t)i*HDIM+c];
-      #pragma unroll
-      for (int r=0;r<4;r++) f4fma(acc[r], et4[r][i], w);
-    }
-    #pragma unroll
-    for (int r=0;r<4;r++) *(float4*)&bufA[half*4096 + (ks*4+r)*HDIM + c] = acc[r];
-  }
-  __syncthreads();
-  {
-    int h=t&255, rh=t>>8;
-    float bd = db1[h], bf = fb1[h], fw = fW2[h];
-    float val[2];
-    #pragma unroll
-    for (int rr=0;rr<2;rr++){
-      int r = 2*rh+rr;
-      float sd=0.f, sf=0.f;
-      #pragma unroll
-      for (int k=0;k<4;k++){ sd += bufA[(k*4+r)*HDIM+h]; sf += bufA[4096+(k*4+r)*HDIM+h]; }
-      hd4[r][h] = fmaxf(sd+bd, 0.f);
-      val[rr] = fmaxf(sf+bf, 0.f)*fw;
-    }
-    #pragma unroll
-    for (int s2=32;s2>0;s2>>=1){
-      val[0] += __shfl_xor(val[0], s2, 64);
-      val[1] += __shfl_xor(val[1], s2, 64);
-    }
-    if (lane==0){ wred[wid*2]=val[0]; wred[wid*2+1]=val[1]; }
-  }
-  __syncthreads();
-  {
-    int r_ = t>>7, rem = t&127, k_ = rem&7, j_ = rem>>3;
-    float lp = 0.f;
-    #pragma unroll 4
-    for (int i=0;i<16;i++){
-      int h = j_ + 16*i;
-      lp += hd4[r_][h]*w2s[h*KK + k_];
-    }
-    redsm[t] = lp;
-  }
-  __syncthreads();
-  if (wid == 0 && lane < 32){
-    int r = lane>>3, k = lane&7;
-    int base = (r>=2)?4:0, off = r&1;
-    float fs = 0.f;
-    #pragma unroll
-    for (int w=0;w<4;w++) fs += wred[(base+w)*2 + off];
-    float fac = 1.f/(1.f+expf(-(fs+fb2[0])));
-    float s = db2[k] + g[(size_t)(e0+r)*KK + k];
-    #pragma unroll
-    for (int j=0;j<16;j++) s += redsm[r*128 + j*8 + k];
-    float z = s*2.0f;
-    float m = z;
-    m = fmaxf(m, __shfl_xor(m, 1, 64));
-    m = fmaxf(m, __shfl_xor(m, 2, 64));
-    m = fmaxf(m, __shfl_xor(m, 4, 64));
-    float pz = expf(z - m);
-    float sum = pz;
-    sum += __shfl_xor(sum, 1, 64);
-    sum += __shfl_xor(sum, 2, 64);
-    sum += __shfl_xor(sum, 4, 64);
-    fdv[r][k] = fac * pz / sum;
-  }
-  __syncthreads();
-  {
-    int d = t&127, r = t>>7;
-    float a = 0.f;
-    #pragma unroll
-    for (int k=0;k<KK;k++) a += fdv[r][k]*type_emb[(size_t)k*DD + d];
-    et4[r][d] = a;
-    ete_g[(size_t)(e0+r)*DD + d] = a;
-  }
-  __syncthreads();
-  {
-    float4 acc[4];
-    #pragma unroll
-    for (int r=0;r<4;r++) acc[r]=make_float4(0.f,0.f,0.f,0.f);
-    #pragma unroll
-    for (int i=0;i<16;i++){
-      int idx = ksW*16 + i;
-      #pragma unroll
-      for (int r=0;r<4;r++) f4fma(acc[r], et4[r][idx], wreg[i]);
-    }
-    #pragma unroll
-    for (int r=0;r<4;r++) *(float4*)&bufA[(ksW*4+r)*HDIM + cW] = acc[r];
-  }
-  __syncthreads();
-  {
-    int h=t&255, rh=t>>8;
-    float bv = wb1[h];
-    #pragma unroll
-    for (int rr=0;rr<2;rr++){
-      int r = 2*rh+rr;
+      for (int i=ks1*64;i<ks1*64+64;i++){
+        float4 w = *(const float4*)&oW1[(size_t)i*HDIM+c1];
+        f4fma(acc[0], agflC[0*512+i], w);
+        f4fma(acc[1], agflC[1*512+i], w);
+      }
+      #pragma unroll
+      for (int r=0;r<2;r++) *(float4*)&partC[(ks1*2+r)*HDIM+c1]=acc[r];
+    }
+    __syncthreads();
+    {
+      int h=t&255, r=t>>8;
       float s=0.f;
       #pragma unroll
-      for (int k=0;k<8;k++) s += bufA[(k*4+r)*HDIM + h];
-      hd4[r][h] = s + bv;
-    }
-  }
-  __syncthreads();
-  {
-    int n = t&255, hh = t>>8;
-    const float4* Vrow = (const float4*)(Vm + ((size_t)(b*NN)+n)*HDIM);
-    float acc[4]={0.f,0.f,0.f,0.f};
-    #pragma unroll 4
-    for (int ii=hh*32; ii<hh*32+32; ii++){
-      float4 v = Vrow[ii];
-      float w0=w2l[4*ii+0], w1=w2l[4*ii+1], wc=w2l[4*ii+2], w3=w2l[4*ii+3];
-      #pragma unroll
-      for (int r=0;r<4;r++){
-        acc[r] += fmaxf(hd4[r][4*ii+0]+v.x,0.f)*w0
-                + fmaxf(hd4[r][4*ii+1]+v.y,0.f)*w1
-                + fmaxf(hd4[r][4*ii+2]+v.z,0.f)*wc
-                + fmaxf(hd4[r][4*ii+3]+v.w,0.f)*w3;
-      }
-    }
-    #pragma unroll
-    for (int r=0;r<4;r++) bufA[(hh*4+r)*256 + n] = acc[r];
-  }
-  __syncthreads();
-  if (wid < 4){
-    int r = wid;
-    float b2v = wb2[0];
-    float c0 = c0p[0];
-    float x[4]; bool msk[4];
-    #pragma unroll
-    for (int q=0;q<4;q++){
-      int n = lane + 64*q;
-      msk[q] = (Hm[(size_t)(e0+r)*NN + n] != 0.f);
-      float raw = msk[q] ? (bufA[(0*4+r)*256+n] + bufA[(1*4+r)*256+n] + b2v) : c0;
-      x[q] = raw>0.f ? raw : 0.01f*raw;
-    }
-    float m = fmaxf(fmaxf(x[0],x[1]), fmaxf(x[2],x[3]));
-    #pragma unroll
-    for (int s2=32;s2>0;s2>>=1) m = fmaxf(m, __shfl_xor(m, s2, 64));
-    float p[4]; float ss=0.f;
-    #pragma unroll
-    for (int q=0;q<4;q++){ p[q]=expf(x[q]-m); ss+=p[q]; }
-    #pragma unroll
-    for (int s2=32;s2>0;s2>>=1) ss += __shfl_xor(ss, s2, 64);
-    float inv = 1.f/ss;
-    #pragma unroll
-    for (int q=0;q<4;q++){
-      int n = lane + 64*q;
-      bufA[2048 + r*256 + n] = msk[q] ? p[q]*inv : 0.f;
-    }
-  }
-  __syncthreads();
-  if (t < 256){
-    int n = t;
-    float4 o4;
-    o4.x = bufA[2048 + 0*256 + n];
-    o4.y = bufA[2048 + 1*256 + n];
-    o4.z = bufA[2048 + 2*256 + n];
-    o4.w = bufA[2048 + 3*256 + n];
-    int eb = e0 & 511;
-    *(float4*)(HwT + ((size_t)(b*NN)+n)*EE + eb) = o4;
-  }
-}
-
-__global__ __launch_bounds__(512) void agent_kernel(
-                             const float* HwT, const float* edgef, const float* ete,
-                             const float* af,
-                             const float* qW, const float* qb, const float* iqW, const float* iqb,
-                             const float* k2, const float* v2,
-                             const float* op_W, const float* op_b,
-                             const float* oW1, const float* ob1,
-                             const float* oW2, const float* ob2,
-                             float* pnew, float* anew){
-  __shared__ int   ecomp[2][EE];
-  __shared__ float wcomp[2][EE];
-  __shared__ int   wcnt[2][4];
-  __shared__ float agfl[2][512];
-  __shared__ float part[4096];
-  __shared__ float Qs[2][DD];
-  __shared__ float qr[2][DD];
-  __shared__ float att[2][4][PP+1];
-  __shared__ float o_l[2][DD];
-  __shared__ float hid[2][HDIM];
-  int n0 = blockIdx.x*2; int b = n0 >> 8; int t = threadIdx.x;
-  int tt = t & 255, rr = t >> 8;
-  int lane = t & 63, wid = t >> 6;
-  int lw = tt >> 6;
-
-  {
-    int bn = n0 + rr;
-    const float* wrow = HwT + (size_t)bn*EE;
-    int total = 0;
-    #pragma unroll
-    for (int p=0;p<2;p++){
-      int e = p*256 + tt;
-      float w = wrow[e];
-      bool pred = (w != 0.f);
-      unsigned long long mask = __ballot(pred);
-      if (lane==0) wcnt[rr][lw] = __popcll(mask);
-      int off = __popcll(mask & ((1ull<<lane)-1ull));
-      __syncthreads();
-      int wb = total;
-      for (int ww=0; ww<lw; ww++) wb += wcnt[rr][ww];
-      if (pred){ ecomp[rr][wb+off] = e; wcomp[rr][wb+off] = w; }
-      total += wcnt[rr][0]+wcnt[rr][1]+wcnt[rr][2]+wcnt[rr][3];
-      __syncthreads();
-    }
-    float acc = 0.f;
-    const float* srcbase = (tt < DD) ? (edgef + (size_t)b*EE*DD + tt)
-                                     : (ete   + (size_t)b*EE*DD + (tt-DD));
-    for (int i=0;i<total;i++){
-      acc += wcomp[rr][i] * srcbase[(size_t)ecomp[rr][i]*DD];
-    }
-    agfl[rr][tt] = acc;
-    if (tt < DD) agfl[rr][2*DD+tt] = af[(size_t)bn*DD + tt];
-  }
-  __syncthreads();
-  int c=(tt&31)*4, ps=tt>>5;
-  {
-    float4 a = make_float4(0.f,0.f,0.f,0.f);
-    #pragma unroll 4
-    for (int i=ps*48;i<ps*48+48;i++){
-      float4 w = *(const float4*)&qW[(size_t)i*DD+c];
-      f4fma(a, agfl[rr][i], w);
-    }
-    *(float4*)&part[(rr*8+ps)*DD+c]=a;
-  }
-  __syncthreads();
-  if (t<256){
-    int cc=t&127, r=t>>7;
-    float s=0.f;
-    #pragma unroll
-    for (int k=0;k<8;k++) s+=part[(r*8+k)*DD+cc];
-    Qs[r][cc]=s+qb[cc];
-  }
-  __syncthreads();
-  {
-    float4 a = make_float4(0.f,0.f,0.f,0.f);
-    #pragma unroll 4
-    for (int i=ps*16;i<ps*16+16;i++){
-      float4 w = *(const float4*)&iqW[(size_t)i*DD+c];
-      f4fma(a, Qs[rr][i], w);
-    }
-    *(float4*)&part[(rr*8+ps)*DD+c]=a;
-  }
-  __syncthreads();
-  if (t<256){
-    int cc=t&127, r=t>>7;
-    float s=0.f;
-    #pragma unroll
-    for (int k=0;k<8;k++) s+=part[(r*8+k)*DD+cc];
-    qr[r][cc]=s+iqb[cc];
-  }
-  __syncthreads();
-  const float scale = 0.17677669529663687f;
-  {
-    const float* krow = k2 + ((size_t)(b*PP) + tt)*DD;
-    #pragma unroll
-    for (int hh=0;hh<2;hh++){
-      int h = rr*2+hh;
-      const float4* k4 = (const float4*)(krow + h*32);
-      float s0=0.f, s1=0.f;
-      #pragma unroll
-      for (int jj=0;jj<8;jj++){
-        float4 kk = k4[jj];
-        s0 += qr[0][h*32+jj*4+0]*kk.x + qr[0][h*32+jj*4+1]*kk.y
-            + qr[0][h*32+jj*4+2]*kk.z + qr[0][h*32+jj*4+3]*kk.w;
-        s1 += qr[1][h*32+jj*4+0]*kk.x + qr[1][h*32+jj*4+1]*kk.y
-            + qr[1][h*32+jj*4+2]*kk.z + qr[1][h*32+jj*4+3]*kk.w;
-      }
-      att[0][h][tt] = s0*scale;
-      att[1][h][tt] = s1*scale;
-    }
-  }
-  __syncthreads();
-  {
-    int r = wid>>2, h = wid&3;
-    float v0 = att[r][h][lane],     v1 = att[r][h][lane+64],
-          ve = att[r][h][lane+128], v3 = att[r][h][lane+192];
-    float m = fmaxf(fmaxf(v0,v1), fmaxf(ve,v3));
-    #pragma unroll
-    for (int s2=32;s2>0;s2>>=1) m = fmaxf(m, __shfl_xor(m, s2, 64));
-    float e0 = expf(v0-m), e1 = expf(v1-m), e2 = expf(ve-m), e3 = expf(v3-m);
-    float ss = (e0+e1)+(e2+e3);
-    #pragma unroll
-    for (int s2=32;s2>0;s2>>=1) ss += __shfl_xor(ss, s2, 64);
-    float inv = 1.f/ss;
-    att[r][h][lane] = e0*inv; att[r][h][lane+64] = e1*inv;
-    att[r][h][lane+128] = e2*inv; att[r][h][lane+192] = e3*inv;
-  }
-  __syncthreads();
-  int h2 = c >> 5;
-  {
-    float4 acc = make_float4(0.f,0.f,0.f,0.f);
-    #pragma unroll 4
-    for (int i=0;i<32;i++){
-      int p = ps*32+i;
-      float4 v = *(const float4*)&v2[((size_t)(b*PP)+p)*DD + c];
-      f4fma(acc, att[rr][h2][p], v);
-    }
-    *(float4*)&part[(rr*8+ps)*DD+c]=acc;
-  }
-  __syncthreads();
-  if (t<256){
-    int cc=t&127, r=t>>7;
-    float s=0.f;
-    #pragma unroll
-    for (int k=0;k<8;k++) s+=part[(r*8+k)*DD+cc];
-    o_l[r][cc]=s;
-  }
-  __syncthreads();
-  {
-    float4 a2 = make_float4(0.f,0.f,0.f,0.f);
-    #pragma unroll 4
-    for (int i=ps*16;i<ps*16+16;i++){
-      float4 w = *(const float4*)&op_W[(size_t)i*DD + c];
-      f4fma(a2, o_l[rr][i], w);
-    }
-    *(float4*)&part[(rr*8+ps)*DD+c]=a2;
-  }
-  __syncthreads();
-  if (t<256){
-    int cc=t&127, r=t>>7;
-    float s=0.f;
-    #pragma unroll
-    for (int k=0;k<8;k++) s+=part[(r*8+k)*DD+cc];
-    float pv = s+op_b[cc];
-    agfl[r][3*DD+cc] = pv;
-    pnew[(size_t)(n0+r)*DD+cc] = pv;
-  }
-  __syncthreads();
-  {
-    int c1=(t&63)*4, ks1=t>>6;
-    float4 acc[2];
-    #pragma unroll
-    for (int r=0;r<2;r++) acc[r]=make_float4(0.f,0.f,0.f,0.f);
-    #pragma unroll 8
-    for (int i=ks1*64;i<ks1*64+64;i++){
-      float4 w = *(const float4*)&oW1[(size_t)i*HDIM+c1];
-      f4fma(acc[0], agfl[0][i], w);
-      f4fma(acc[1], agfl[1][i], w);
-    }
-    #pragma unroll
-    for (int r=0;r<2;r++) *(float4*)&part[(ks1*2+r)*HDIM+c1]=acc[r];
-  }
-  __syncthreads();
-  {
-    int h=t&255, r=t>>8;
-    float s=0.f;
-    #pragma unroll
-    for (int k=0;k<8;k++) s+=part[(k*2+r)*HDIM+h];
-    hid[r][h] = fmaxf(s+ob1[h], 0.f);
-  }
-  __syncthreads();
-  {
-    float4 a2 = make_float4(0.f,0.f,0.f,0.f);
-    #pragma unroll 8
-    for (int h=ps*32;h<ps*32+32;h++){
-      float4 w = *(const float4*)&oW2[(size_t)h*DD+c];
-      f4fma(a2, hid[rr][h], w);
-    }
-    *(float4*)&part[(rr*8+ps)*DD+c]=a2;
-  }
-  __syncthreads();
-  if (t<256){
-    int cc=t&127, r=t>>7;
-    float s=0.f;
-    #pragma unroll
-    for (int k=0;k<8;k++) s+=part[(r*8+k)*DD+cc];
-    anew[(size_t)(n0+r)*DD+cc]=s+ob2[cc];
+      for (int k=0;k<8;k++) s+=partC[(k*2+r)*HDIM+h];
+      hidC[r*HDIM+h] = fmaxf(s+ob1[h], 0.f);
+    }
+    __syncthreads();
+    {
+      float4 a2 = make_float4(0.f,0.f,0.f,0.f);
+      #pragma unroll 8
+      for (int h=ps*32;h<ps*32+32;h++){
+        float4 w = *(const float4*)&oW2[(size_t)h*DD+c];
+        f4fma(a2, hidC[rr*HDIM+h], w);
+      }
+      *(float4*)&partC[(rr*8+ps)*DD+c]=a2;
+    }
+    __syncthreads();
+    if (t<256){
+      int cc=t&127, r=t>>7;
+      float s=0.f;
+      #pragma unroll
+      for (int k=0;k<8;k++) s+=partC[(r*8+k)*DD+cc];
+      anew[(size_t)(n0+r)*DD+cc]=s+ob2[cc];
+    }
   }
 }
 
@@ -791,22 +728,18 @@
   float* out  = (float*)d_out;
   float* anew = out;
   float* pnew = out + BB*NN*DD;
-
-  prep_kernel<<<PB_END, 256, 0, stream>>>(
-      ws+WS_G, ws+WS_C0, w_b1, w_W2, w_b2,
-      Hm, af, at, w_W1, w_b1,
-      ws+WS_U1, ws+WS_ETYPE, ws+WS_V,
-      pf, k_W,k_b,ik_W,ik_b, v_W,v_b,iv_W,iv_b,
-      ws+WS_K2, ws+WS_V2);
-  edge_kernel<<<256,512,0,stream>>>(
-      Hm, af, ws+WS_V, ws+WS_U1, ws+WS_ETYPE,
+  int* cnt = (int*)(ws + WS_CNT);
+
+  hipMemsetAsync((void*)cnt, 0, 64, stream);
+  fused_kernel<<<256, 512, 0, stream>>>(
+      af, at, pf, Hm, type_emb,
       w_W1, w_b1, w_W2, w_b2,
-      d_W1,d_b1,d_W2,d_b2, f_W1,f_b1,f_W2,f_b2,
-      type_emb, ws+WS_G, ws+WS_C0,
-      ws+WS_EDGEF, ws+WS_ETE, ws+WS_HWT);
-  agent_kernel<<<256,512,0,stream>>>(
-      ws+WS_HWT, ws+WS_EDGEF, ws+WS_ETE, af,
-      q_W, q_b, iq_W, iq_b,
-      ws+WS_K2, ws+WS_V2, op_W, op_b,
-      o_W1,o_b1,o_W2,o_b2, pnew, anew);
+      d_W1, d_b1, d_W2, d_b2,
+      f_W1, f_b1, f_W2, f_b2,
+      o_W1, o_b1, o_W2, o_b2,
+      q_W, q_b, k_W, k_b, v_W, v_b,
+      iq_W, iq_b, ik_W, ik_b, iv_W, iv_b,
+      op_W, op_b,
+      ws+WS_V, ws+WS_EDGEF, ws+WS_ETE, ws+WS_HWT,
+      ws+WS_K2, ws+WS_V2, cnt, pnew, anew);
 }
```

Measured after the change: 183.7 us. +106.2%, slower.
